# Performance work log

Measured on AMD Instinct MI355X. Metric: run time of the kernel, lower is better.

Reference implementation:

```python
import jax, jax.numpy as jnp
import numpy as np

B, L, C, H, W = 2, 3, 64, 32, 32
DI, N, DT_RANK, K = 128, 16, 4, 4  # d_inner=2*C, d_state, dt_rank=ceil(C/16), 4 scan dirs


def setup_inputs() -> dict:
    key = jax.random.key(0)
    ks = iter(jax.random.split(key, 48))
    nrm = lambda shape, s=0.02: jax.random.normal(next(ks), shape, jnp.float32) * s
    return {
        "image_sequence": jax.random.normal(next(ks), (B, L, C, H, W), jnp.float32),
        "difficult_zone": jax.random.normal(next(ks), (B, C, H, W), jnp.float32),
        "sigma": jax.random.uniform(next(ks), (B, C, H, W), jnp.float32),
        # LayerNorm2d applied to each frame
        "norm_g": jnp.ones((C,)), "norm_b": jnp.zeros((C,)),
        # ConvolutionalResBlock (in=3C -> out=C), GroupNorm(num_groups=1)
        "gn1_g": jnp.ones((3 * C,)), "gn1_b": jnp.zeros((3 * C,)),
        "conv1_w": nrm((C, 3 * C, 3, 3)), "conv1_b": jnp.zeros((C,)),
        "gn2_g": jnp.ones((C,)), "gn2_b": jnp.zeros((C,)),
        "conv2_w": nrm((C, C, 3, 3)), "conv2_b": jnp.zeros((C,)),
        "skip_w": nrm((C, 3 * C, 1, 1)), "skip_b": jnp.zeros((C,)),
        # VSSBlock pre-norms
        "ln1_g": jnp.ones((C,)), "ln1_b": jnp.zeros((C,)),
        "ln2_g": jnp.ones((C,)), "ln2_b": jnp.zeros((C,)),
        # SS2D
        "in_proj_w": nrm((2 * DI, C)),
        "dwconv_w": nrm((DI, 1, 3, 3)), "dwconv_b": jnp.zeros((DI,)),
        "x_proj_w": nrm((K, DT_RANK + 2 * N, DI)),
        "dt_proj_w": nrm((K, DI, DT_RANK), 0.1),
        "dt_proj_b": jnp.log(jnp.expm1(jnp.full((K, DI), 0.01, jnp.float32))),
        "A_logs": jnp.log(jnp.tile(jnp.arange(1, N + 1, dtype=jnp.float32), (K * DI, 1))),
        "Ds": jnp.ones((K * DI,)),
        "out_norm_g": jnp.ones((DI,)), "out_norm_b": jnp.zeros((DI,)),
        "out_proj_w": nrm((C, DI)),
        # Mlp (hidden = C)
        "fc1_w": nrm((C, C)), "fc1_b": jnp.zeros((C,)),
        "fc2_w": nrm((C, C)), "fc2_b": jnp.zeros((C,)),
    }


def _ln(x, g, b, eps=1e-5):  # layernorm over last axis
    m = x.mean(-1, keepdims=True)
    v = x.var(-1, keepdims=True)
    return (x - m) * jax.lax.rsqrt(v + eps) * g + b


def _ln2d(x, g, b, eps=1e-6):  # per-pixel channel layernorm, NCHW
    m = x.mean(1, keepdims=True)
    v = x.var(1, keepdims=True)
    return (x - m) * jax.lax.rsqrt(v + eps) * g[None, :, None, None] + b[None, :, None, None]


def _gn1(x, g, b, eps=1e-5):  # GroupNorm(num_groups=1), NCHW
    m = x.mean((1, 2, 3), keepdims=True)
    v = x.var((1, 2, 3), keepdims=True)
    return (x - m) * jax.lax.rsqrt(v + eps) * g[None, :, None, None] + b[None, :, None, None]


def _conv(x, w, b, pad):
    y = jax.lax.conv_general_dilated(x, w, (1, 1), [(pad, pad), (pad, pad)],
                                     dimension_numbers=("NCHW", "OIHW", "NCHW"))
    return y + b[None, :, None, None]


def _forward(image_sequence, difficult_zone, sigma, norm_g, norm_b, gn1_g, gn1_b,
             conv1_w, conv1_b, gn2_g, gn2_b, conv2_w, conv2_b, skip_w, skip_b,
             ln1_g, ln1_b, ln2_g, ln2_b, in_proj_w, dwconv_w, dwconv_b, x_proj_w,
             dt_proj_w, dt_proj_b, A_logs, Ds, out_norm_g, out_norm_b, out_proj_w,
             fc1_w, fc1_b, fc2_w, fc2_b):
    b, l, c, h, w = image_sequence.shape
    bl, L2 = b * l, h * w
    # fold frame loop into batch (identical math per frame in the torch loop)
    frames = _ln2d(image_sequence.reshape(bl, c, h, w), norm_g, norm_b)
    dz = jnp.broadcast_to(difficult_zone[:, None], (b, l, c, h, w)).reshape(bl, c, h, w)
    sg = jnp.broadcast_to(sigma[:, None], (b, l, c, h, w)).reshape(bl, c, h, w)
    x = jnp.concatenate([dz, frames, sg], axis=1)  # [bl, 3c, h, w]
    # channel compressor: pre-act conv res block
    hdn = _conv(jax.nn.silu(_gn1(x, gn1_g, gn1_b)), conv1_w, conv1_b, 1)
    hdn = _conv(jax.nn.silu(_gn1(hdn, gn2_g, gn2_b)), conv2_w, conv2_b, 1)
    x = hdn + _conv(x, skip_w, skip_b, 0)          # [bl, c, h, w]
    x = x.transpose(0, 2, 3, 1)                    # [bl, h, w, c]
    # --- VSSBlock (pre-norm): x = x + SS2D(LN(x)) ---
    xn = _ln(x, ln1_g, ln1_b)
    xz = xn @ in_proj_w.T                          # [bl,h,w,2*DI]
    xc, z = jnp.split(xz, 2, axis=-1)
    xc = xc.transpose(0, 3, 1, 2)                  # [bl, DI, h, w]
    xc = jax.lax.conv_general_dilated(xc, dwconv_w, (1, 1), [(1, 1), (1, 1)],
                                      dimension_numbers=("NCHW", "OIHW", "NCHW"),
                                      feature_group_count=DI) + dwconv_b[None, :, None, None]
    xc = jax.nn.silu(xc)
    # 4-direction scan inputs (HW, WH, and their reverses)
    xf = xc.reshape(bl, DI, L2)
    xt = xc.transpose(0, 1, 3, 2).reshape(bl, DI, L2)
    xs = jnp.stack([xf, xt], axis=1)
    xs = jnp.concatenate([xs, jnp.flip(xs, axis=-1)], axis=1)  # [bl, 4, DI, L2]
    x_dbl = jnp.einsum("bkdl,kcd->bkcl", xs, x_proj_w)
    dts, Bs, Cs = jnp.split(x_dbl, [DT_RANK, DT_RANK + N], axis=2)
    dts = jnp.einsum("bkrl,kdr->bkdl", dts, dt_proj_w) + dt_proj_b[None, :, :, None]
    dts = jax.nn.softplus(dts)                     # [bl, 4, DI, L2]
    A = -jnp.exp(A_logs).reshape(K, DI, N)
    dA = jnp.exp(dts[..., None] * A[None, :, :, None, :])            # [bl,4,DI,L2,N]
    dBu = dts[..., None] * Bs.transpose(0, 1, 3, 2)[:, :, None] * xs[..., None]
    a_t = dA.transpose(3, 0, 1, 2, 4)              # [L2, bl, 4, DI, N]
    bu_t = dBu.transpose(3, 0, 1, 2, 4)
    c_t = Cs.transpose(3, 0, 1, 2)                 # [L2, bl, 4, N]

    def step(hid, inp):
        a_i, bu_i, c_i = inp
        hid = a_i * hid + bu_i
        return hid, jnp.einsum("bkdn,bkn->bkd", hid, c_i)

    h0 = jnp.zeros((bl, K, DI, N), xs.dtype)
    _, ys = jax.lax.scan(step, h0, (a_t, bu_t, c_t))                 # [L2, bl, 4, DI]
    ys = ys.transpose(1, 2, 3, 0) + xs * Ds.reshape(K, DI)[None, :, :, None]
    inv = jnp.flip(ys[:, 2:4], axis=-1)
    y = (ys[:, 0] + inv[:, 0]
         + ys[:, 1].reshape(bl, DI, w, h).transpose(0, 1, 3, 2).reshape(bl, DI, L2)
         + inv[:, 1].reshape(bl, DI, w, h).transpose(0, 1, 3, 2).reshape(bl, DI, L2))
    y = _ln(y.transpose(0, 2, 1), out_norm_g, out_norm_b).reshape(bl, h, w, DI)
    y = y * jax.nn.silu(z)
    x = x + y @ out_proj_w.T
    # --- x = x + Mlp(LN(x)) ---
    xn = _ln(x, ln2_g, ln2_b)
    x = x + (jax.nn.gelu(xn @ fc1_w.T + fc1_b, approximate=False) @ fc2_w.T + fc2_b)
    return x.transpose(0, 3, 1, 2).reshape(b, l, c, h, w)


def reference(image_sequence, difficult_zone, sigma, norm_g, norm_b, gn1_g, gn1_b,
              conv1_w, conv1_b, gn2_g, gn2_b, conv2_w, conv2_b, skip_w, skip_b,
              ln1_g, ln1_b, ln2_g, ln2_b, in_proj_w, dwconv_w, dwconv_b, x_proj_w,
              dt_proj_w, dt_proj_b, A_logs, Ds, out_norm_g, out_norm_b, out_proj_w,
              fc1_w, fc1_b, fc2_w, fc2_b):
    return _forward(image_sequence, difficult_zone, sigma, norm_g, norm_b, gn1_g, gn1_b,
                    conv1_w, conv1_b, gn2_g, gn2_b, conv2_w, conv2_b, skip_w, skip_b,
                    ln1_g, ln1_b, ln2_g, ln2_b, in_proj_w, dwconv_w, dwconv_b, x_proj_w,
                    dt_proj_w, dt_proj_b, A_logs, Ds, out_norm_g, out_norm_b, out_proj_w,
                    fc1_w, fc1_b, fc2_w, fc2_b)
```

## Files before the change

### kernel.cpp

```cpp
#include <hip/hip_runtime.h>
#include <math.h>

#define BL    6
#define CCH   64
#define C3    192
#define L2    1024
#define DIC   128
#define NST   16
#define K4    4
#define PSTR  1088
#define NCH   32

#define LOG2E 1.44269504088896340736f
#define LN2C  0.69314718055994530942f

__device__ __forceinline__ float fexp(float x){ return __builtin_amdgcn_exp2f(x*LOG2E); }
__device__ __forceinline__ float fsilu(float x){ return x / (1.f + fexp(-x)); }
__device__ __forceinline__ float fsoftplus(float x){
  if (x > 20.f) return x;
  return __builtin_amdgcn_logf(1.f + fexp(x)) * LN2C;
}
__device__ __forceinline__ float fgelu(float x){
  return 0.5f*x*(1.f + erff(x*0.70710678118654752440f));
}

__global__ __launch_bounds__(256) void k_ln2d(const float* __restrict__ img,
    const float* __restrict__ dz, const float* __restrict__ sg,
    const float* __restrict__ g, const float* __restrict__ b, float* __restrict__ x3c,
    float* __restrict__ psum1, float* __restrict__ psq1){
  __shared__ float ps[4][64], pq[4][64];
  int s = blockIdx.x >> 4;
  int lane = threadIdx.x & 63;
  int cg = threadIdx.x >> 6;
  int p = ((blockIdx.x & 15) << 6) + lane;
  int bsmp = s/3;
  const float* fr = img + (size_t)s*CCH*L2;
  float vals[16]; float sm=0.f, sq=0.f;
  #pragma unroll
  for (int j=0;j<16;++j){
    int c = cg*16+j;
    float v = fr[c*L2+p];
    vals[j]=v; sm+=v; sq+=v*v;
  }
  ps[cg][lane]=sm; pq[cg][lane]=sq;
  __syncthreads();
  sm = ps[0][lane]+ps[1][lane]+ps[2][lane]+ps[3][lane];
  sq = pq[0][lane]+pq[1][lane]+pq[2][lane]+pq[3][lane];
  float mean = sm*(1.f/CCH); float var = sq*(1.f/CCH) - mean*mean;
  float rs = rsqrtf(var + 1e-6f);
  float* o = x3c + (size_t)s*C3*L2;
  const float* dzp = dz + (size_t)bsmp*CCH*L2;
  const float* sgp = sg + (size_t)bsmp*CCH*L2;
  float gsm=0.f, gsq=0.f;
  #pragma unroll
  for (int j=0;j<16;++j){
    int c = cg*16+j;
    float dzv = dzp[c*L2+p];
    float nv  = (vals[j]-mean)*rs*g[c] + b[c];
    float sgv = sgp[c*L2+p];
    o[c*L2+p] = dzv;
    o[(CCH+c)*L2+p] = nv;
    o[(2*CCH+c)*L2+p] = sgv;
    gsm += dzv+nv+sgv; gsq += dzv*dzv+nv*nv+sgv*sgv;
  }
  for (int m=1;m<64;m<<=1){ gsm+=__shfl_xor(gsm,m,64); gsq+=__shfl_xor(gsq,m,64); }
  __syncthreads();
  if (lane==0){ ps[cg][0]=gsm; pq[cg][0]=gsq; }
  __syncthreads();
  if (threadIdx.x==0){
    atomicAdd(psum1+s, ps[0][0]+ps[1][0]+ps[2][0]+ps[3][0]);
    atomicAdd(psq1 +s, pq[0][0]+pq[1][0]+pq[2][0]+pq[3][0]);
  }
}

__global__ __launch_bounds__(256) void k_gnact_pad(const float* __restrict__ x,
    const float* __restrict__ psum, const float* __restrict__ psq,
    const float* __restrict__ g, const float* __restrict__ b,
    int ch, float inv_n, float eps, float* __restrict__ out){
  int bx = blockIdx.x;
  int s = bx / ch; int c = bx % ch;
  int tid = threadIdx.x;
  float mean = psum[s]*inv_n;
  float var = psq[s]*inv_n - mean*mean;
  float rs = rsqrtf(var + eps);
  float gc = g[c]*rs; float bc = b[c] - mean*rs*g[c];
  float4 v = *(const float4*)(x + (size_t)bx*1024 + tid*4);
  float4 o; o.x = fsilu(v.x*gc+bc); o.y = fsilu(v.y*gc+bc);
  o.z = fsilu(v.z*gc+bc); o.w = fsilu(v.w*gc+bc);
  float* pl = out + (size_t)bx*PSTR;
  *(float4*)(pl + 32 + tid*4) = o;
  float4 z4 = make_float4(0.f,0.f,0.f,0.f);
  if (tid < 8)  *(float4*)(pl + tid*4) = z4;
  else if (tid < 16) *(float4*)(pl + 1056 + (tid-8)*4) = z4;
}

__device__ __forceinline__ void conv_row_acc(float4& a0, float4& a1, float4 mid, float lf, float rt,
    const float* wp0, const float* wp1){
  float w0=wp0[0], w1=wp0[1], w2=wp0[2];
  a0.x = fmaf(w0,lf,   fmaf(w1,mid.x, fmaf(w2,mid.y, a0.x)));
  a0.y = fmaf(w0,mid.x,fmaf(w1,mid.y, fmaf(w2,mid.z, a0.y)));
  a0.z = fmaf(w0,mid.y,fmaf(w1,mid.z, fmaf(w2,mid.w, a0.z)));
  a0.w = fmaf(w0,mid.z,fmaf(w1,mid.w, fmaf(w2,rt,    a0.w)));
  float v0=wp1[0], v1=wp1[1], v2=wp1[2];
  a1.x = fmaf(v0,lf,   fmaf(v1,mid.x, fmaf(v2,mid.y, a1.x)));
  a1.y = fmaf(v0,mid.x,fmaf(v1,mid.y, fmaf(v2,mid.z, a1.y)));
  a1.z = fmaf(v0,mid.y,fmaf(v1,mid.z, fmaf(v2,mid.w, a1.z)));
  a1.w = fmaf(v0,mid.z,fmaf(v1,mid.w, fmaf(v2,rt,    a1.w)));
}

__device__ __forceinline__ void conv_ci_body(float4 m0, float4 m1, float4 m2, int q,
    const float* wp0, const float* wp1, float4& a0, float4& a1){
  float lf0=__shfl_up(m0.w,1,64), rt0=__shfl_down(m0.x,1,64);
  float lf1=__shfl_up(m1.w,1,64), rt1=__shfl_down(m1.x,1,64);
  float lf2=__shfl_up(m2.w,1,64), rt2=__shfl_down(m2.x,1,64);
  if (q==0){ lf0=0.f; lf1=0.f; lf2=0.f; }
  if (q==7){ rt0=0.f; rt1=0.f; rt2=0.f; }
  conv_row_acc(a0,a1,m0,lf0,rt0, wp0+0, wp1+0);
  conv_row_acc(a0,a1,m1,lf1,rt1, wp0+3, wp1+3);
  conv_row_acc(a0,a1,m2,lf2,rt2, wp0+6, wp1+6);
}

__global__ __launch_bounds__(256) void k_conv1_split(const float* __restrict__ xact,
    const float* __restrict__ w, float* __restrict__ part){
  int bx = blockIdx.x; int kk = bx&7; int cop=(bx>>3)&31; int s=bx>>8;
  int co0 = cop*2, co1 = co0+1;
  int tid = threadIdx.x; int row = tid>>3; int q = tid&7; int col0 = q*4;
  float4 a0 = make_float4(0.f,0.f,0.f,0.f);
  float4 a1 = make_float4(0.f,0.f,0.f,0.f);
  int ci0 = kk*24;
  const float* pl = xact + ((size_t)s*C3 + ci0)*PSTR + row*32 + col0;
  const float* wp0 = w + (size_t)(co0*C3 + ci0)*9;
  const float* wp1 = w + (size_t)(co1*C3 + ci0)*9;
  float4 m0 = *(const float4*)(pl);
  float4 m1 = *(const float4*)(pl+32);
  float4 m2 = *(const float4*)(pl+64);
  #pragma unroll 2
  for (int i=0;i<24;++i){
    const float* pn = pl + (i<23 ? PSTR : 0);
    float4 n0 = *(const float4*)(pn);
    float4 n1 = *(const float4*)(pn+32);
    float4 n2 = *(const float4*)(pn+64);
    conv_ci_body(m0,m1,m2,q, wp0, wp1, a0, a1);
    wp0 += 9; wp1 += 9; pl = pn; m0=n0; m1=n1; m2=n2;
  }
  float* pp = part + (size_t)kk*(BL*CCH*L2) + ((size_t)s*CCH+co0)*L2 + row*32+col0;
  *(float4*)pp = a0;
  *(float4*)(pp+L2) = a1;
}

__global__ __launch_bounds__(256) void k_reduce1(const float* __restrict__ part,
    const float* __restrict__ bias, float* __restrict__ h1,
    float* __restrict__ psum2, float* __restrict__ psq2){
  int co = blockIdx.x & 63; int s = blockIdx.x >> 6;
  size_t ofs = ((size_t)s*CCH+co)*L2 + threadIdx.x*4;
  const size_t stride = (size_t)BL*CCH*L2;
  float4 acc = *(const float4*)(part + ofs);
  #pragma unroll
  for (int kk=1;kk<8;++kk){
    float4 r = *(const float4*)(part + (size_t)kk*stride + ofs);
    acc.x += r.x; acc.y += r.y; acc.z += r.z; acc.w += r.w;
  }
  float bv = bias[co];
  acc.x += bv; acc.y += bv; acc.z += bv; acc.w += bv;
  *(float4*)(h1 + ofs) = acc;
  float sm = acc.x+acc.y+acc.z+acc.w;
  float sq = acc.x*acc.x+acc.y*acc.y+acc.z*acc.z+acc.w*acc.w;
  for (int m=1;m<64;m<<=1){ sm+=__shfl_xor(sm,m,64); sq+=__shfl_xor(sq,m,64); }
  __shared__ float s_sm[4], s_sq[4];
  int wv = threadIdx.x>>6;
  if ((threadIdx.x&63)==0){ s_sm[wv]=sm; s_sq[wv]=sq; }
  __syncthreads();
  if (threadIdx.x==0){
    atomicAdd(psum2+s, s_sm[0]+s_sm[1]+s_sm[2]+s_sm[3]);
    atomicAdd(psq2 +s, s_sq[0]+s_sq[1]+s_sq[2]+s_sq[3]);
  }
}

__global__ __launch_bounds__(256) void k_conv2_split(const float* __restrict__ xact2,
    const float* __restrict__ x3c, const float* __restrict__ w2,
    const float* __restrict__ wsk, float* __restrict__ part){
  int t = blockIdx.x; int role = t % 3; t /= 3;
  int cop = t & 31; int s = t >> 5;
  int co0 = cop*2, co1 = co0+1;
  int tid = threadIdx.x; int row = tid>>3; int q = tid&7; int col0 = q*4;
  int p = row*32+col0;
  float4 a0 = make_float4(0.f,0.f,0.f,0.f);
  float4 a1 = make_float4(0.f,0.f,0.f,0.f);
  if (role < 2){
    int ci0 = role*32;
    const float* pl = xact2 + ((size_t)s*CCH + ci0)*PSTR + row*32 + col0;
    const float* wp0 = w2 + (size_t)(co0*CCH + ci0)*9;
    const float* wp1 = w2 + (size_t)(co1*CCH + ci0)*9;
    float4 m0 = *(const float4*)(pl);
    float4 m1 = *(const float4*)(pl+32);
    float4 m2 = *(const float4*)(pl+64);
    #pragma unroll 2
    for (int i=0;i<32;++i){
      const float* pn = pl + (i<31 ? PSTR : 0);
      float4 n0 = *(const float4*)(pn);
      float4 n1 = *(const float4*)(pn+32);
      float4 n2 = *(const float4*)(pn+64);
      conv_ci_body(m0,m1,m2,q, wp0, wp1, a0, a1);
      wp0 += 9; wp1 += 9; pl = pn; m0=n0; m1=n1; m2=n2;
    }
  } else {
    const float* x3 = x3c + (size_t)s*C3*L2 + p;
    #pragma unroll 4
    for (int ci=0; ci<C3; ++ci){
      float4 v = *(const float4*)(x3 + (size_t)ci*L2);
      float ws0 = wsk[co0*C3+ci], ws1 = wsk[co1*C3+ci];
      a0.x = fmaf(ws0,v.x,a0.x); a0.y = fmaf(ws0,v.y,a0.y); a0.z = fmaf(ws0,v.z,a0.z); a0.w = fmaf(ws0,v.w,a0.w);
      a1.x = fmaf(ws1,v.x,a1.x); a1.y = fmaf(ws1,v.y,a1.y); a1.z = fmaf(ws1,v.z,a1.z); a1.w = fmaf(ws1,v.w,a1.w);
    }
  }
  float* pp = part + (size_t)role*(BL*CCH*L2) + ((size_t)s*CCH+co0)*L2 + p;
  *(float4*)pp = a0;
  *(float4*)(pp+L2) = a1;
}

__global__ __launch_bounds__(256) void k_reduce2(const float* __restrict__ part,
    const float* __restrict__ b2, const float* __restrict__ bsk,
    float* __restrict__ xp, float* __restrict__ x_cmaj){
  int co = blockIdx.x & 63; int s = blockIdx.x >> 6;
  int p = threadIdx.x*4;
  size_t ofs = ((size_t)s*CCH+co)*L2 + p;
  const size_t stride = (size_t)BL*CCH*L2;
  float4 r0 = *(const float4*)(part + ofs);
  float4 r1 = *(const float4*)(part + stride + ofs);
  float4 r2 = *(const float4*)(part + 2*stride + ofs);
  float bv = b2[co]+bsk[co];
  float4 o;
  o.x = r0.x+r1.x+r2.x+bv;
  o.y = r0.y+r1.y+r2.y+bv;
  o.z = r0.z+r1.z+r2.z+bv;
  o.w = r0.w+r1.w+r2.w+bv;
  *(float4*)(x_cmaj + ofs) = o;
  float* xpb = xp + ((size_t)s*L2 + p)*CCH + co;
  xpb[0] = o.x; xpb[CCH] = o.y; xpb[2*CCH] = o.z; xpb[3*CCH] = o.w;
}

__global__ __launch_bounds__(256) void k_ln1_inproj(const float* __restrict__ xp,
    const float* __restrict__ g, const float* __restrict__ b, const float* __restrict__ W,
    float* __restrict__ xc, float* __restrict__ z_t){
  __shared__ float xn_s[64*65];
  int bx = blockIdx.x; int oq = bx & 3; int pg = (bx>>2)&15; int s = bx>>6;
  int p0 = pg*64;
  int tid = threadIdx.x; int wv = __builtin_amdgcn_readfirstlane(tid>>6); int lane = tid&63;
  for (int j=0;j<16;++j){
    int pl = wv*16 + j; int p = p0 + pl;
    float v = xp[((size_t)s*L2 + p)*CCH + lane];
    float sm = v, sq = v*v;
    for (int m=1;m<64;m<<=1){ sm += __shfl_xor(sm,m,64); sq += __shfl_xor(sq,m,64); }
    float mean = sm*(1.f/64.f); float var = sq*(1.f/64.f) - mean*mean;
    float rs = rsqrtf(var + 1e-5f);
    xn_s[pl*65 + lane] = (v-mean)*rs*g[lane] + b[lane];
  }
  __syncthreads();
  int px_l = tid & 63;
  int og = __builtin_amdgcn_readfirstlane(tid >> 6);
  int o0 = oq*64 + og*16;
  float acc[16];
  #pragma unroll
  for (int oi=0;oi<16;++oi) acc[oi]=0.f;
  for (int c=0;c<64;++c){
    float xv = xn_s[px_l*65 + c];
    #pragma unroll
    for (int oi=0;oi<16;++oi) acc[oi] = fmaf(W[(o0+oi)*64 + c], xv, acc[oi]);
  }
  int p = p0 + px_l;
  if (oq < 2){
    #pragma unroll
    for (int oi=0;oi<16;++oi) xc[((size_t)s*DIC + o0 + oi)*L2 + p] = acc[oi];
  } else {
    #pragma unroll
    for (int oi=0;oi<16;++oi) z_t[((size_t)s*DIC + (o0-128) + oi)*L2 + p] = acc[oi];
  }
}

__global__ __launch_bounds__(256) void k_dwconv(const float* __restrict__ xc,
    const float* __restrict__ w, const float* __restrict__ bias, float* __restrict__ xconv){
  int bx = blockIdx.x; int dch = bx & 127; int s = bx >> 7;
  int tid = threadIdx.x; int row = tid>>3; int q = tid&7; int col0 = q*4;
  const float* xr = xc + ((size_t)s*DIC+dch)*L2;
  const float* wp = w + dch*9;
  float bv = bias[dch];
  float4 acc = make_float4(bv,bv,bv,bv);
  #pragma unroll
  for (int dy=-1;dy<=1;++dy){
    int r = row+dy;
    float4 mid = make_float4(0.f,0.f,0.f,0.f);
    if (0<=r && r<32) mid = *(const float4*)(xr + r*32 + col0);
    float lf = __shfl_up(mid.w,1,64); if(q==0) lf=0.f;
    float rt = __shfl_down(mid.x,1,64); if(q==7) rt=0.f;
    float w0=wp[(dy+1)*3], w1=wp[(dy+1)*3+1], w2=wp[(dy+1)*3+2];
    acc.x = fmaf(w0,lf,   fmaf(w1,mid.x, fmaf(w2,mid.y, acc.x)));
    acc.y = fmaf(w0,mid.x,fmaf(w1,mid.y, fmaf(w2,mid.z, acc.y)));
    acc.z = fmaf(w0,mid.y,fmaf(w1,mid.z, fmaf(w2,mid.w, acc.z)));
    acc.w = fmaf(w0,mid.z,fmaf(w1,mid.w, fmaf(w2,rt,    acc.w)));
  }
  acc.x = fsilu(acc.x); acc.y = fsilu(acc.y); acc.z = fsilu(acc.z); acc.w = fsilu(acc.w);
  *(float4*)(xconv + ((size_t)s*DIC+dch)*L2 + row*32+col0) = acc;
}

__global__ __launch_bounds__(256) void k_xproj_dt(const float* __restrict__ xconv,
    const float* __restrict__ W, const float* __restrict__ dtw, const float* __restrict__ dtb,
    float* __restrict__ dtp, float* __restrict__ Bp, float* __restrict__ Cp,
    float* __restrict__ u_t){
  __shared__ float smem[128*68];
  int bx = blockIdx.x; int pg = bx & 15; int sk = bx >> 4;
  int k = sk & 3; int s = sk >> 2;
  int tid = threadIdx.x;
  for (int i = tid; i < 128*16; i += 256){
    int dr = i>>4; int j4 = (i&15)*4;
    float4 v = *(const float4*)(xconv + ((size_t)(s*DIC + dr))*L2 + pg*64 + j4);
    *(float4*)&smem[dr*68 + j4] = v;
  }
  __syncthreads();
  if (k == 0){
    float* ub = u_t + ((size_t)(s*L2) + pg*64)*DIC;
    for (int i = tid; i < 64*128; i += 256){
      int px2 = i>>7; int dd = i&127;
      ub[(size_t)px2*DIC + dd] = smem[dd*68 + px2];
    }
  }
  int px = tid & 63;
  int cgrp = __builtin_amdgcn_readfirstlane(tid >> 6);
  int c0 = cgrp*9;
  const float* wb = W + (size_t)(k*36 + c0)*DIC;
  float acc[9];
  #pragma unroll
  for (int ci=0;ci<9;++ci) acc[ci]=0.f;
  for (int d=0; d<DIC; ++d){
    float xv = smem[d*68 + px];
    #pragma unroll
    for (int ci=0;ci<9;++ci) acc[ci] = fmaf(wb[ci*DIC+d], xv, acc[ci]);
  }
  __syncthreads();
  #pragma unroll
  for (int ci=0;ci<9;++ci) smem[(c0+ci)*68 + px] = acc[ci];
  __syncthreads();
  int d = tid & 127; int half = tid >> 7;
  float w0 = dtw[(k*DIC+d)*4+0], w1 = dtw[(k*DIC+d)*4+1];
  float w2 = dtw[(k*DIC+d)*4+2], w3 = dtw[(k*DIC+d)*4+3];
  float bb = dtb[k*DIC+d];
  float* dout = dtp + ((size_t)sk*L2 + pg*64)*DIC + d;
  for (int pp = half*32; pp < half*32+32; ++pp){
    float r0 = smem[0*68+pp], r1 = smem[1*68+pp], r2 = smem[2*68+pp], r3 = smem[3*68+pp];
    float val = fsoftplus(fmaf(w0,r0,fmaf(w1,r1,fmaf(w2,r2,fmaf(w3,r3,bb)))));
    dout[(size_t)pp*DIC] = val;
  }
  float* Bb = Bp + ((size_t)sk*L2 + pg*64)*NST;
  float* Cb = Cp + ((size_t)sk*L2 + pg*64)*NST;
  for (int i = tid; i < 1024; i += 256){
    int pp = i>>4; int n = i&15;
    Bb[pp*NST + n] = smem[(4+n)*68 + pp];
    Cb[pp*NST + n] = smem[(20+n)*68 + pp];
  }
}

__device__ __forceinline__ int scan_pix32(int ch, int j, int k){
  if (k==0) return ch*32 + j;
  if (k==1) return j*32 + ch;
  if (k==2) return 1023 - (ch*32 + j);
  return 1023 - (j*32 + ch);
}

struct StepB { float dtv, uv; float4 B0,B1,B2,B3; };
__device__ __forceinline__ StepB loadB(const float* db, const float* ub, const float* Bb, int p){
  StepB r;
  r.dtv = db[(size_t)p*DIC]; r.uv = ub[(size_t)p*DIC];
  const float* bp = Bb + p*NST;
  r.B0 = *(const float4*)bp; r.B1 = *(const float4*)(bp+4);
  r.B2 = *(const float4*)(bp+8); r.B3 = *(const float4*)(bp+12);
  return r;
}

__global__ __launch_bounds__(256,2) void k_scan_part3(const float* __restrict__ dtp,
    const float* __restrict__ u_t, const float* __restrict__ Bp,
    const float* __restrict__ A_logs, float* __restrict__ hend, float* __restrict__ prodA){
  int bx = blockIdx.x; int chp = bx & 15; int sk = bx >> 4;
  int k = sk & 3; int s = sk >> 2;
  int tid = threadIdx.x; int d = tid & 127; int ch = chp*2 + (tid>>7);
  float aco[16];
  {
    const float* ab = A_logs + (size_t)(k*DIC+d)*NST;
    #pragma unroll
    for (int n=0;n<16;++n) aco[n] = -LOG2E * fexp(ab[n]);
  }
  float h[16], Pr[16];
  #pragma unroll
  for (int n=0;n<16;++n){ h[n]=0.f; Pr[n]=1.f; }
  const float* db = dtp + (size_t)sk*L2*DIC + d;
  const float* ub = u_t + (size_t)s*L2*DIC + d;
  const float* Bb = Bp + (size_t)sk*L2*NST;
  StepB cur = loadB(db, ub, Bb, scan_pix32(ch, 0, k));
  #pragma unroll 4
  for (int j=0;j<32;++j){
    StepB nxt;
    if (j < 31) nxt = loadB(db, ub, Bb, scan_pix32(ch, j+1, k));
    float tv = cur.dtv*cur.uv;
    #define PSTEP(NI, BV) { float a_ = __builtin_amdgcn_exp2f(cur.dtv*aco[NI]); \
      h[NI] = fmaf(a_, h[NI], tv*(BV)); Pr[NI] *= a_; }
    PSTEP(0,cur.B0.x) PSTEP(1,cur.B0.y) PSTEP(2,cur.B0.z) PSTEP(3,cur.B0.w)
    PSTEP(4,cur.B1.x) PSTEP(5,cur.B1.y) PSTEP(6,cur.B1.z) PSTEP(7,cur.B1.w)
    PSTEP(8,cur.B2.x) PSTEP(9,cur.B2.y) PSTEP(10,cur.B2.z) PSTEP(11,cur.B2.w)
    PSTEP(12,cur.B3.x) PSTEP(13,cur.B3.y) PSTEP(14,cur.B3.z) PSTEP(15,cur.B3.w)
    #undef PSTEP
    cur = nxt;
  }
  size_t base = ((size_t)(sk*NCH + ch)*DIC + d)*NST;
  #pragma unroll
  for (int q4=0;q4<4;++q4){
    *(float4*)(hend + base + q4*4)  = make_float4(h[q4*4],h[q4*4+1],h[q4*4+2],h[q4*4+3]);
    *(float4*)(prodA + base + q4*4) = make_float4(Pr[q4*4],Pr[q4*4+1],Pr[q4*4+2],Pr[q4*4+3]);
  }
}

__global__ __launch_bounds__(256) void k_scan_fix3(const float* __restrict__ hend,
    float* prodA_Hin){
  int t = blockIdx.x*256 + threadIdx.x;
  int n = t & 15; int d = (t>>4) & 127; int sk = t >> 11;
  float H = 0.f;
  for (int ch=0; ch<NCH; ++ch){
    size_t idx = ((size_t)(sk*NCH + ch)*DIC + d)*NST + n;
    float pa = prodA_Hin[idx];
    float he = hend[idx];
    prodA_Hin[idx] = H;
    H = fmaf(pa, H, he);
  }
}

__global__ __launch_bounds__(256,2) void k_scan_y3(const float* __restrict__ dtp,
    const float* __restrict__ u_t, const float* __restrict__ Bp, const float* __restrict__ Cp,
    const float* __restrict__ A_logs, const float* __restrict__ Ds,
    const float* __restrict__ Hin, float* __restrict__ ys_t){
  int bx = blockIdx.x; int chp = bx & 15; int sk = bx >> 4;
  int k = sk & 3; int s = sk >> 2;
  int tid = threadIdx.x; int d = tid & 127; int ch = chp*2 + (tid>>7);
  float aco[16];
  {
    const float* ab = A_logs + (size_t)(k*DIC+d)*NST;
    #pragma unroll
    for (int n=0;n<16;++n) aco[n] = -LOG2E * fexp(ab[n]);
  }
  float Dv = Ds[k*DIC+d];
  float h[16];
  size_t hbase = ((size_t)(sk*NCH + ch)*DIC + d)*NST;
  #pragma unroll
  for (int q4=0;q4<4;++q4){
    float4 hv = *(const float4*)(Hin + hbase + q4*4);
    h[q4*4]=hv.x; h[q4*4+1]=hv.y; h[q4*4+2]=hv.z; h[q4*4+3]=hv.w;
  }
  const float* db = dtp + (size_t)sk*L2*DIC + d;
  const float* ub = u_t + (size_t)s*L2*DIC + d;
  const float* Bb = Bp + (size_t)sk*L2*NST;
  const float* Cb = Cp + (size_t)sk*L2*NST;
  float* yb = ys_t + (size_t)sk*L2*DIC + d;
  int pcur = scan_pix32(ch, 0, k);
  StepB cur = loadB(db, ub, Bb, pcur);
  float4 Cc0 = *(const float4*)(Cb + pcur*NST);
  float4 Cc1 = *(const float4*)(Cb + pcur*NST + 4);
  float4 Cc2 = *(const float4*)(Cb + pcur*NST + 8);
  float4 Cc3 = *(const float4*)(Cb + pcur*NST + 12);
  #pragma unroll 4
  for (int j=0;j<32;++j){
    StepB nxt; float4 Cn0, Cn1, Cn2, Cn3; int pn = pcur;
    if (j < 31){
      pn = scan_pix32(ch, j+1, k);
      nxt = loadB(db, ub, Bb, pn);
      Cn0 = *(const float4*)(Cb + pn*NST);
      Cn1 = *(const float4*)(Cb + pn*NST + 4);
      Cn2 = *(const float4*)(Cb + pn*NST + 8);
      Cn3 = *(const float4*)(Cb + pn*NST + 12);
    }
    float tv = cur.dtv*cur.uv;
    float y0=0.f, y1=0.f, y2=0.f, y3=0.f;
    #define YSTEP(NI, BV, CV, YA) { float a_ = __builtin_amdgcn_exp2f(cur.dtv*aco[NI]); \
      h[NI] = fmaf(a_, h[NI], tv*(BV)); YA = fmaf(h[NI], (CV), YA); }
    YSTEP(0,cur.B0.x,Cc0.x,y0) YSTEP(1,cur.B0.y,Cc0.y,y1) YSTEP(2,cur.B0.z,Cc0.z,y2) YSTEP(3,cur.B0.w,Cc0.w,y3)
    YSTEP(4,cur.B1.x,Cc1.x,y0) YSTEP(5,cur.B1.y,Cc1.y,y1) YSTEP(6,cur.B1.z,Cc1.z,y2) YSTEP(7,cur.B1.w,Cc1.w,y3)
    YSTEP(8,cur.B2.x,Cc2.x,y0) YSTEP(9,cur.B2.y,Cc2.y,y1) YSTEP(10,cur.B2.z,Cc2.z,y2) YSTEP(11,cur.B2.w,Cc2.w,y3)
    YSTEP(12,cur.B3.x,Cc3.x,y0) YSTEP(13,cur.B3.y,Cc3.y,y1) YSTEP(14,cur.B3.z,Cc3.z,y2) YSTEP(15,cur.B3.w,Cc3.w,y3)
    #undef YSTEP
    yb[(size_t)pcur*DIC] = fmaf(cur.uv, Dv, (y0+y1)+(y2+y3));
    cur = nxt; Cc0 = Cn0; Cc1 = Cn1; Cc2 = Cn2; Cc3 = Cn3; pcur = pn;
  }
}

__global__ __launch_bounds__(256) void k_combine_outproj(const float* __restrict__ ys_t,
    const float* __restrict__ z_t, const float* __restrict__ g, const float* __restrict__ b,
    const float* __restrict__ W, const float* __restrict__ x_cmaj, float* __restrict__ xv){
  __shared__ float yt[128*17];
  int s = blockIdx.x >> 6; int pg = blockIdx.x & 63;
  int tid = threadIdx.x;
  int wv = __builtin_amdgcn_readfirstlane(tid>>6); int lane = tid&63;
  int d0 = lane, d1 = lane+64;
  for (int i=0;i<4;++i){
    int px = i*4 + wv; int p = pg*16 + px;
    const float* yb = ys_t + ((size_t)(s*4)*L2 + p)*DIC;
    float ya = yb[d0] + yb[(size_t)L2*DIC + d0] + yb[(size_t)2*L2*DIC + d0] + yb[(size_t)3*L2*DIC + d0];
    float yc = yb[d1] + yb[(size_t)L2*DIC + d1] + yb[(size_t)2*L2*DIC + d1] + yb[(size_t)3*L2*DIC + d1];
    float sm = ya+yc, sq = ya*ya+yc*yc;
    for (int m=1;m<64;m<<=1){ sm+=__shfl_xor(sm,m,64); sq+=__shfl_xor(sq,m,64); }
    float mean = sm*(1.f/128.f); float var = sq*(1.f/128.f)-mean*mean;
    float rs = rsqrtf(var + 1e-5f);
    float yn0 = (ya-mean)*rs*g[d0] + b[d0];
    float yn1 = (yc-mean)*rs*g[d1] + b[d1];
    float zv0 = z_t[((size_t)s*DIC+d0)*L2 + p];
    float zv1 = z_t[((size_t)s*DIC+d1)*L2 + p];
    yt[d0*17 + px] = yn0 * fsilu(zv0);
    yt[d1*17 + px] = yn1 * fsilu(zv1);
  }
  __syncthreads();
  int px = tid & 15; int cg = tid >> 4;
  int c0 = cg*4;
  float a0=0.f,a1=0.f,a2=0.f,a3=0.f;
  for (int d=0; d<DIC; ++d){
    float yv = yt[d*17 + px];
    a0 = fmaf(W[(c0+0)*DIC + d], yv, a0);
    a1 = fmaf(W[(c0+1)*DIC + d], yv, a1);
    a2 = fmaf(W[(c0+2)*DIC + d], yv, a2);
    a3 = fmaf(W[(c0+3)*DIC + d], yv, a3);
  }
  int p = pg*16 + px;
  size_t base = ((size_t)s*CCH + c0)*L2 + p;
  xv[base]      = x_cmaj[base]      + a0;
  xv[base+L2]   = x_cmaj[base+L2]   + a1;
  xv[base+2*L2] = x_cmaj[base+2*L2] + a2;
  xv[base+3*L2] = x_cmaj[base+3*L2] + a3;
}

__global__ __launch_bounds__(256) void k_mlp(const float* __restrict__ xv_in,
    const float* __restrict__ g, const float* __restrict__ b,
    const float* __restrict__ w1, const float* __restrict__ b1,
    const float* __restrict__ w2, const float* __restrict__ b2, float* __restrict__ out){
  __shared__ float xt[64*33];
  __shared__ float ts[32*65];
  int s = blockIdx.x >> 5; int p0 = (blockIdx.x & 31)*32;
  int tid = threadIdx.x; int px = tid & 31; int cg = tid >> 5;
  #pragma unroll
  for (int j=0;j<8;++j){
    int c = cg*8 + j;
    xt[c*33 + px] = xv_in[((size_t)s*CCH + c)*L2 + p0 + px];
  }
  __syncthreads();
  float sm=0.f, sq=0.f;
  for (int c=0;c<64;++c){ float v = xt[c*33+px]; sm+=v; sq+=v*v; }
  float mean = sm*(1.f/64.f);
  float rs = rsqrtf(sq*(1.f/64.f) - mean*mean + 1e-5f);
  int o0 = cg*8;
  float t[8];
  #pragma unroll
  for (int oi=0;oi<8;++oi) t[oi] = b1[o0+oi];
  for (int c=0;c<64;++c){
    float xn = (xt[c*33+px]-mean)*rs*g[c] + b[c];
    #pragma unroll
    for (int oi=0;oi<8;++oi) t[oi] = fmaf(xn, w1[(o0+oi)*64 + c], t[oi]);
  }
  #pragma unroll
  for (int oi=0;oi<8;++oi) ts[px*65 + o0+oi] = fgelu(t[oi]);
  __syncthreads();
  int c0 = cg*8;
  float acc[8];
  #pragma unroll
  for (int ci=0;ci<8;++ci) acc[ci] = xt[(c0+ci)*33+px] + b2[c0+ci];
  for (int o=0;o<64;++o){
    float tv = ts[px*65 + o];
    #pragma unroll
    for (int ci=0;ci<8;++ci) acc[ci] = fmaf(tv, w2[(c0+ci)*64 + o], acc[ci]);
  }
  #pragma unroll
  for (int ci=0;ci<8;++ci) out[((size_t)s*CCH + c0+ci)*L2 + p0 + px] = acc[ci];
}

extern "C" void kernel_launch(void* const* d_in, const int* in_sizes, int n_in,
                              void* d_out, int out_size, void* d_ws, size_t ws_size,
                              hipStream_t stream){
  (void)in_sizes; (void)n_in; (void)out_size; (void)ws_size;
  const float* img      = (const float*)d_in[0];
  const float* dz       = (const float*)d_in[1];
  const float* sg       = (const float*)d_in[2];
  const float* norm_g   = (const float*)d_in[3];
  const float* norm_b   = (const float*)d_in[4];
  const float* gn1_g    = (const float*)d_in[5];
  const float* gn1_b    = (const float*)d_in[6];
  const float* conv1_w  = (const float*)d_in[7];
  const float* conv1_b  = (const float*)d_in[8];
  const float* gn2_g    = (const float*)d_in[9];
  const float* gn2_b    = (const float*)d_in[10];
  const float* conv2_w  = (const float*)d_in[11];
  const float* conv2_b  = (const float*)d_in[12];
  const float* skip_w   = (const float*)d_in[13];
  const float* skip_b   = (const float*)d_in[14];
  const float* ln1_g    = (const float*)d_in[15];
  const float* ln1_b    = (const float*)d_in[16];
  const float* ln2_g    = (const float*)d_in[17];
  const float* ln2_b    = (const float*)d_in[18];
  const float* in_proj_w= (const float*)d_in[19];
  const float* dwconv_w = (const float*)d_in[20];
  const float* dwconv_b = (const float*)d_in[21];
  const float* x_proj_w = (const float*)d_in[22];
  const float* dt_proj_w= (const float*)d_in[23];
  const float* dt_proj_b= (const float*)d_in[24];
  const float* A_logs   = (const float*)d_in[25];
  const float* Ds       = (const float*)d_in[26];
  const float* out_norm_g = (const float*)d_in[27];
  const float* out_norm_b = (const float*)d_in[28];
  const float* out_proj_w = (const float*)d_in[29];
  const float* fc1_w    = (const float*)d_in[30];
  const float* fc1_b    = (const float*)d_in[31];
  const float* fc2_w    = (const float*)d_in[32];
  const float* fc2_b    = (const float*)d_in[33];

  float* ws = (float*)d_ws;
  float* x3c    = ws;
  float* xact1  = x3c    + 1179648;
  float* h1     = xact1  + 1253376;
  float* xact2  = h1     + 393216;
  float* xp     = xact2  + 417792;
  float* x_cmaj = xp     + 393216;
  float* z_t    = x_cmaj + 393216;
  float* xc     = z_t    + 786432;
  float* xconv  = xc     + 786432;
  float* hole   = xconv  + 786432;
  float* dtp    = hole   + 884736;
  float* ys_t   = dtp    + 3145728;
  float* xv     = ys_t   + 3145728;
  float* statsb = xv     + 393216;
  float* psum1  = statsb;
  float* psq1   = statsb + 6;
  float* psum2  = statsb + 12;
  float* psq2   = statsb + 18;
  float* part1  = dtp;
  float* part2  = ys_t;
  float* hend   = x3c;
  float* prodA  = xconv;
  float* u_t    = h1;
  float* Bp     = xp;
  float* Cp     = xc;

  hipMemsetAsync(statsb, 0, 24*sizeof(float), stream);
  k_ln2d<<<96, 256, 0, stream>>>(img, dz, sg, norm_g, norm_b, x3c, psum1, psq1);
  k_gnact_pad<<<6*C3, 256, 0, stream>>>(x3c, psum1, psq1, gn1_g, gn1_b, C3,
                                        1.f/(C3*L2), 1e-5f, xact1);
  k_conv1_split<<<1536, 256, 0, stream>>>(xact1, conv1_w, part1);
  k_reduce1<<<384, 256, 0, stream>>>(part1, conv1_b, h1, psum2, psq2);
  k_gnact_pad<<<6*CCH, 256, 0, stream>>>(h1, psum2, psq2, gn2_g, gn2_b, CCH,
                                         1.f/(CCH*L2), 1e-5f, xact2);
  k_conv2_split<<<576, 256, 0, stream>>>(xact2, x3c, conv2_w, skip_w, part2);
  k_reduce2<<<384, 256, 0, stream>>>(part2, conv2_b, skip_b, xp, x_cmaj);
  k_ln1_inproj<<<384, 256, 0, stream>>>(xp, ln1_g, ln1_b, in_proj_w, xc, z_t);
  k_dwconv<<<768, 256, 0, stream>>>(xc, dwconv_w, dwconv_b, xconv);
  k_xproj_dt<<<384, 256, 0, stream>>>(xconv, x_proj_w, dt_proj_w, dt_proj_b, dtp, Bp, Cp, u_t);
  k_scan_part3<<<384, 256, 0, stream>>>(dtp, u_t, Bp, A_logs, hend, prodA);
  k_scan_fix3<<<192, 256, 0, stream>>>(hend, prodA);
  k_scan_y3<<<384, 256, 0, stream>>>(dtp, u_t, Bp, Cp, A_logs, Ds, prodA, ys_t);
  k_combine_outproj<<<384, 256, 0, stream>>>(ys_t, z_t, out_norm_g, out_norm_b,
                                             out_proj_w, x_cmaj, xv);
  k_mlp<<<192, 256, 0, stream>>>(xv, ln2_g, ln2_b, fc1_w, fc1_b, fc2_w, fc2_b, (float*)d_out);
}
```

Measured before the change: 316.8 us.

## Fuse all stages into one cooperative persistent kernel with grid syncs

Turns every stage function into a device function and runs them all from a single cooperative mega-kernel. Each stage loops over its virtual blocks, and stages are separated by grid-wide barriers, with the grid capped at 512 blocks. The aim is to remove the launch overhead and inter-kernel gaps of fifteen launches. In exchange, every stage gets the same register and LDS footprint and fewer resident blocks, and grid.sync itself has a cost. If the cooperative launch fails, the code falls back to per-stage kernels.

```diff
diff --git a/kernel.cpp b/kernel.cpp
--- a/kernel.cpp
+++ b/kernel.cpp
@@ -1,5 +1,8 @@
 #include <hip/hip_runtime.h>
+#include <hip/hip_cooperative_groups.h>
 #include <math.h>
+
+namespace cg = cooperative_groups;
 
 #define BL    6
 #define CCH   64
@@ -24,75 +27,17 @@
   return 0.5f*x*(1.f + erff(x*0.70710678118654752440f));
 }
 
-__global__ __launch_bounds__(256) void k_ln2d(const float* __restrict__ img,
-    const float* __restrict__ dz, const float* __restrict__ sg,
-    const float* __restrict__ g, const float* __restrict__ b, float* __restrict__ x3c,
-    float* __restrict__ psum1, float* __restrict__ psq1){
-  __shared__ float ps[4][64], pq[4][64];
-  int s = blockIdx.x >> 4;
-  int lane = threadIdx.x & 63;
-  int cg = threadIdx.x >> 6;
-  int p = ((blockIdx.x & 15) << 6) + lane;
-  int bsmp = s/3;
-  const float* fr = img + (size_t)s*CCH*L2;
-  float vals[16]; float sm=0.f, sq=0.f;
-  #pragma unroll
-  for (int j=0;j<16;++j){
-    int c = cg*16+j;
-    float v = fr[c*L2+p];
-    vals[j]=v; sm+=v; sq+=v*v;
-  }
-  ps[cg][lane]=sm; pq[cg][lane]=sq;
-  __syncthreads();
-  sm = ps[0][lane]+ps[1][lane]+ps[2][lane]+ps[3][lane];
-  sq = pq[0][lane]+pq[1][lane]+pq[2][lane]+pq[3][lane];
-  float mean = sm*(1.f/CCH); float var = sq*(1.f/CCH) - mean*mean;
-  float rs = rsqrtf(var + 1e-6f);
-  float* o = x3c + (size_t)s*C3*L2;
-  const float* dzp = dz + (size_t)bsmp*CCH*L2;
-  const float* sgp = sg + (size_t)bsmp*CCH*L2;
-  float gsm=0.f, gsq=0.f;
-  #pragma unroll
-  for (int j=0;j<16;++j){
-    int c = cg*16+j;
-    float dzv = dzp[c*L2+p];
-    float nv  = (vals[j]-mean)*rs*g[c] + b[c];
-    float sgv = sgp[c*L2+p];
-    o[c*L2+p] = dzv;
-    o[(CCH+c)*L2+p] = nv;
-    o[(2*CCH+c)*L2+p] = sgv;
-    gsm += dzv+nv+sgv; gsq += dzv*dzv+nv*nv+sgv*sgv;
-  }
-  for (int m=1;m<64;m<<=1){ gsm+=__shfl_xor(gsm,m,64); gsq+=__shfl_xor(gsq,m,64); }
-  __syncthreads();
-  if (lane==0){ ps[cg][0]=gsm; pq[cg][0]=gsq; }
-  __syncthreads();
-  if (threadIdx.x==0){
-    atomicAdd(psum1+s, ps[0][0]+ps[1][0]+ps[2][0]+ps[3][0]);
-    atomicAdd(psq1 +s, pq[0][0]+pq[1][0]+pq[2][0]+pq[3][0]);
-  }
-}
-
-__global__ __launch_bounds__(256) void k_gnact_pad(const float* __restrict__ x,
-    const float* __restrict__ psum, const float* __restrict__ psq,
-    const float* __restrict__ g, const float* __restrict__ b,
-    int ch, float inv_n, float eps, float* __restrict__ out){
-  int bx = blockIdx.x;
-  int s = bx / ch; int c = bx % ch;
-  int tid = threadIdx.x;
-  float mean = psum[s]*inv_n;
-  float var = psq[s]*inv_n - mean*mean;
-  float rs = rsqrtf(var + eps);
-  float gc = g[c]*rs; float bc = b[c] - mean*rs*g[c];
-  float4 v = *(const float4*)(x + (size_t)bx*1024 + tid*4);
-  float4 o; o.x = fsilu(v.x*gc+bc); o.y = fsilu(v.y*gc+bc);
-  o.z = fsilu(v.z*gc+bc); o.w = fsilu(v.w*gc+bc);
-  float* pl = out + (size_t)bx*PSTR;
-  *(float4*)(pl + 32 + tid*4) = o;
-  float4 z4 = make_float4(0.f,0.f,0.f,0.f);
-  if (tid < 8)  *(float4*)(pl + tid*4) = z4;
-  else if (tid < 16) *(float4*)(pl + 1056 + (tid-8)*4) = z4;
-}
+struct MegaP {
+  const float *img,*dz,*sg,*norm_g,*norm_b,*gn1_g,*gn1_b,*conv1_w,*conv1_b,
+              *gn2_g,*gn2_b,*conv2_w,*conv2_b,*skip_w,*skip_b,*ln1_g,*ln1_b,
+              *ln2_g,*ln2_b,*in_proj_w,*dwconv_w,*dwconv_b,*x_proj_w,
+              *dt_proj_w,*dt_proj_b,*A_logs,*Ds,*out_norm_g,*out_norm_b,
+              *out_proj_w,*fc1_w,*fc1_b,*fc2_w,*fc2_b;
+  float *x3c,*xact1,*h1,*xact2,*xp,*x_cmaj,*z_t,*xc,*xconv,*dtp,*ys_t,*xv;
+  float *psum1,*psq1,*psum2,*psq2;
+  float *part1,*part2,*hend,*prodA,*u_t,*Bp,*Cp;
+  float *out;
+};
 
 __device__ __forceinline__ void conv_row_acc(float4& a0, float4& a1, float4 mid, float lf, float rt,
     const float* wp0, const float* wp1){
@@ -120,17 +65,100 @@
   conv_row_acc(a0,a1,m2,lf2,rt2, wp0+6, wp1+6);
 }
 
-__global__ __launch_bounds__(256) void k_conv1_split(const float* __restrict__ xact,
-    const float* __restrict__ w, float* __restrict__ part){
-  int bx = blockIdx.x; int kk = bx&7; int cop=(bx>>3)&31; int s=bx>>8;
+__device__ __forceinline__ int scan_pix32(int ch, int j, int k){
+  if (k==0) return ch*32 + j;
+  if (k==1) return j*32 + ch;
+  if (k==2) return 1023 - (ch*32 + j);
+  return 1023 - (j*32 + ch);
+}
+
+struct StepB { float dtv, uv; float4 B0,B1,B2,B3; };
+__device__ __forceinline__ StepB loadB(const float* db, const float* ub, const float* Bb, int p){
+  StepB r;
+  r.dtv = db[(size_t)p*DIC]; r.uv = ub[(size_t)p*DIC];
+  const float* bp = Bb + p*NST;
+  r.B0 = *(const float4*)bp; r.B1 = *(const float4*)(bp+4);
+  r.B2 = *(const float4*)(bp+8); r.B3 = *(const float4*)(bp+12);
+  return r;
+}
+
+
+__device__ __forceinline__ void p0_ln2d(int vb, int tid, const MegaP& P, float* smem){
+  float* ps = smem;
+  float* pq = smem + 256;
+  int s = vb >> 4;
+  int lane = tid & 63;
+  int cgp = tid >> 6;
+  int p = ((vb & 15) << 6) + lane;
+  int bsmp = s/3;
+  const float* fr = P.img + (size_t)s*CCH*L2;
+  float vals[16]; float sm=0.f, sq=0.f;
+  #pragma unroll
+  for (int j=0;j<16;++j){
+    int c = cgp*16+j;
+    float v = fr[c*L2+p];
+    vals[j]=v; sm+=v; sq+=v*v;
+  }
+  ps[cgp*64+lane]=sm; pq[cgp*64+lane]=sq;
+  __syncthreads();
+  sm = ps[lane]+ps[64+lane]+ps[128+lane]+ps[192+lane];
+  sq = pq[lane]+pq[64+lane]+pq[128+lane]+pq[192+lane];
+  float mean = sm*(1.f/CCH); float var = sq*(1.f/CCH) - mean*mean;
+  float rs = rsqrtf(var + 1e-6f);
+  float* o = P.x3c + (size_t)s*C3*L2;
+  const float* dzp = P.dz + (size_t)bsmp*CCH*L2;
+  const float* sgp = P.sg + (size_t)bsmp*CCH*L2;
+  float gsm=0.f, gsq=0.f;
+  #pragma unroll
+  for (int j=0;j<16;++j){
+    int c = cgp*16+j;
+    float dzv = dzp[c*L2+p];
+    float nv  = (vals[j]-mean)*rs*P.norm_g[c] + P.norm_b[c];
+    float sgv = sgp[c*L2+p];
+    o[c*L2+p] = dzv;
+    o[(CCH+c)*L2+p] = nv;
+    o[(2*CCH+c)*L2+p] = sgv;
+    gsm += dzv+nv+sgv; gsq += dzv*dzv+nv*nv+sgv*sgv;
+  }
+  for (int m=1;m<64;m<<=1){ gsm+=__shfl_xor(gsm,m,64); gsq+=__shfl_xor(gsq,m,64); }
+  __syncthreads();
+  if (lane==0){ ps[cgp*64]=gsm; pq[cgp*64]=gsq; }
+  __syncthreads();
+  if (tid==0){
+    atomicAdd(P.psum1+s, ps[0]+ps[64]+ps[128]+ps[192]);
+    atomicAdd(P.psq1 +s, pq[0]+pq[64]+pq[128]+pq[192]);
+  }
+}
+
+__device__ __forceinline__ void gnact_body(int vb, int tid, const float* __restrict__ x,
+    const float* __restrict__ psum, const float* __restrict__ psq,
+    const float* __restrict__ g, const float* __restrict__ b,
+    int ch, float inv_n, float eps, float* __restrict__ out){
+  int s = vb / ch; int c = vb % ch;
+  float mean = psum[s]*inv_n;
+  float var = psq[s]*inv_n - mean*mean;
+  float rs = rsqrtf(var + eps);
+  float gc = g[c]*rs; float bc = b[c] - mean*rs*g[c];
+  float4 v = *(const float4*)(x + (size_t)vb*1024 + tid*4);
+  float4 o; o.x = fsilu(v.x*gc+bc); o.y = fsilu(v.y*gc+bc);
+  o.z = fsilu(v.z*gc+bc); o.w = fsilu(v.w*gc+bc);
+  float* pl = out + (size_t)vb*PSTR;
+  *(float4*)(pl + 32 + tid*4) = o;
+  float4 z4 = make_float4(0.f,0.f,0.f,0.f);
+  if (tid < 8)  *(float4*)(pl + tid*4) = z4;
+  else if (tid < 16) *(float4*)(pl + 1056 + (tid-8)*4) = z4;
+}
+
+__device__ __forceinline__ void p2_conv1(int vb, int tid, const MegaP& P){
+  int kk = vb&7; int cop=(vb>>3)&31; int s=vb>>8;
   int co0 = cop*2, co1 = co0+1;
-  int tid = threadIdx.x; int row = tid>>3; int q = tid&7; int col0 = q*4;
+  int row = tid>>3; int q = tid&7; int col0 = q*4;
   float4 a0 = make_float4(0.f,0.f,0.f,0.f);
   float4 a1 = make_float4(0.f,0.f,0.f,0.f);
   int ci0 = kk*24;
-  const float* pl = xact + ((size_t)s*C3 + ci0)*PSTR + row*32 + col0;
-  const float* wp0 = w + (size_t)(co0*C3 + ci0)*9;
-  const float* wp1 = w + (size_t)(co1*C3 + ci0)*9;
+  const float* pl = P.xact1 + ((size_t)s*C3 + ci0)*PSTR + row*32 + col0;
+  const float* wp0 = P.conv1_w + (size_t)(co0*C3 + ci0)*9;
+  const float* wp1 = P.conv1_w + (size_t)(co1*C3 + ci0)*9;
   float4 m0 = *(const float4*)(pl);
   float4 m1 = *(const float4*)(pl+32);
   float4 m2 = *(const float4*)(pl+64);
@@ -143,54 +171,50 @@
     conv_ci_body(m0,m1,m2,q, wp0, wp1, a0, a1);
     wp0 += 9; wp1 += 9; pl = pn; m0=n0; m1=n1; m2=n2;
   }
-  float* pp = part + (size_t)kk*(BL*CCH*L2) + ((size_t)s*CCH+co0)*L2 + row*32+col0;
+  float* pp = P.part1 + (size_t)kk*(BL*CCH*L2) + ((size_t)s*CCH+co0)*L2 + row*32+col0;
   *(float4*)pp = a0;
   *(float4*)(pp+L2) = a1;
 }
 
-__global__ __launch_bounds__(256) void k_reduce1(const float* __restrict__ part,
-    const float* __restrict__ bias, float* __restrict__ h1,
-    float* __restrict__ psum2, float* __restrict__ psq2){
-  int co = blockIdx.x & 63; int s = blockIdx.x >> 6;
-  size_t ofs = ((size_t)s*CCH+co)*L2 + threadIdx.x*4;
+__device__ __forceinline__ void p3_reduce1(int vb, int tid, const MegaP& P, float* smem){
+  float* s_sm = smem; float* s_sq = smem+4;
+  int co = vb & 63; int s = vb >> 6;
+  size_t ofs = ((size_t)s*CCH+co)*L2 + tid*4;
   const size_t stride = (size_t)BL*CCH*L2;
-  float4 acc = *(const float4*)(part + ofs);
+  float4 acc = *(const float4*)(P.part1 + ofs);
   #pragma unroll
   for (int kk=1;kk<8;++kk){
-    float4 r = *(const float4*)(part + (size_t)kk*stride + ofs);
+    float4 r = *(const float4*)(P.part1 + (size_t)kk*stride + ofs);
     acc.x += r.x; acc.y += r.y; acc.z += r.z; acc.w += r.w;
   }
-  float bv = bias[co];
+  float bv = P.conv1_b[co];
   acc.x += bv; acc.y += bv; acc.z += bv; acc.w += bv;
-  *(float4*)(h1 + ofs) = acc;
+  *(float4*)(P.h1 + ofs) = acc;
   float sm = acc.x+acc.y+acc.z+acc.w;
   float sq = acc.x*acc.x+acc.y*acc.y+acc.z*acc.z+acc.w*acc.w;
   for (int m=1;m<64;m<<=1){ sm+=__shfl_xor(sm,m,64); sq+=__shfl_xor(sq,m,64); }
-  __shared__ float s_sm[4], s_sq[4];
-  int wv = threadIdx.x>>6;
-  if ((threadIdx.x&63)==0){ s_sm[wv]=sm; s_sq[wv]=sq; }
-  __syncthreads();
-  if (threadIdx.x==0){
-    atomicAdd(psum2+s, s_sm[0]+s_sm[1]+s_sm[2]+s_sm[3]);
-    atomicAdd(psq2 +s, s_sq[0]+s_sq[1]+s_sq[2]+s_sq[3]);
-  }
-}
-
-__global__ __launch_bounds__(256) void k_conv2_split(const float* __restrict__ xact2,
-    const float* __restrict__ x3c, const float* __restrict__ w2,
-    const float* __restrict__ wsk, float* __restrict__ part){
-  int t = blockIdx.x; int role = t % 3; t /= 3;
-  int cop = t & 31; int s = t >> 5;
+  int wv = tid>>6;
+  if ((tid&63)==0){ s_sm[wv]=sm; s_sq[wv]=sq; }
+  __syncthreads();
+  if (tid==0){
+    atomicAdd(P.psum2+s, s_sm[0]+s_sm[1]+s_sm[2]+s_sm[3]);
+    atomicAdd(P.psq2 +s, s_sq[0]+s_sq[1]+s_sq[2]+s_sq[3]);
+  }
+}
+
+__device__ __forceinline__ void p5_conv2(int vb, int tid, const MegaP& P){
+  int t2 = vb; int role = t2 % 3; t2 /= 3;
+  int cop = t2 & 31; int s = t2 >> 5;
   int co0 = cop*2, co1 = co0+1;
-  int tid = threadIdx.x; int row = tid>>3; int q = tid&7; int col0 = q*4;
+  int row = tid>>3; int q = tid&7; int col0 = q*4;
   int p = row*32+col0;
   float4 a0 = make_float4(0.f,0.f,0.f,0.f);
   float4 a1 = make_float4(0.f,0.f,0.f,0.f);
   if (role < 2){
     int ci0 = role*32;
-    const float* pl = xact2 + ((size_t)s*CCH + ci0)*PSTR + row*32 + col0;
-    const float* wp0 = w2 + (size_t)(co0*CCH + ci0)*9;
-    const float* wp1 = w2 + (size_t)(co1*CCH + ci0)*9;
+    const float* pl = P.xact2 + ((size_t)s*CCH + ci0)*PSTR + row*32 + col0;
+    const float* wp0 = P.conv2_w + (size_t)(co0*CCH + ci0)*9;
+    const float* wp1 = P.conv2_w + (size_t)(co1*CCH + ci0)*9;
     float4 m0 = *(const float4*)(pl);
     float4 m1 = *(const float4*)(pl+32);
     float4 m2 = *(const float4*)(pl+64);
@@ -204,56 +228,51 @@
       wp0 += 9; wp1 += 9; pl = pn; m0=n0; m1=n1; m2=n2;
     }
   } else {
-    const float* x3 = x3c + (size_t)s*C3*L2 + p;
+    const float* x3 = P.x3c + (size_t)s*C3*L2 + p;
     #pragma unroll 4
     for (int ci=0; ci<C3; ++ci){
       float4 v = *(const float4*)(x3 + (size_t)ci*L2);
-      float ws0 = wsk[co0*C3+ci], ws1 = wsk[co1*C3+ci];
+      float ws0 = P.skip_w[co0*C3+ci], ws1 = P.skip_w[co1*C3+ci];
       a0.x = fmaf(ws0,v.x,a0.x); a0.y = fmaf(ws0,v.y,a0.y); a0.z = fmaf(ws0,v.z,a0.z); a0.w = fmaf(ws0,v.w,a0.w);
       a1.x = fmaf(ws1,v.x,a1.x); a1.y = fmaf(ws1,v.y,a1.y); a1.z = fmaf(ws1,v.z,a1.z); a1.w = fmaf(ws1,v.w,a1.w);
     }
   }
-  float* pp = part + (size_t)role*(BL*CCH*L2) + ((size_t)s*CCH+co0)*L2 + p;
+  float* pp = P.part2 + (size_t)role*(BL*CCH*L2) + ((size_t)s*CCH+co0)*L2 + p;
   *(float4*)pp = a0;
   *(float4*)(pp+L2) = a1;
 }
 
-__global__ __launch_bounds__(256) void k_reduce2(const float* __restrict__ part,
-    const float* __restrict__ b2, const float* __restrict__ bsk,
-    float* __restrict__ xp, float* __restrict__ x_cmaj){
-  int co = blockIdx.x & 63; int s = blockIdx.x >> 6;
-  int p = threadIdx.x*4;
+__device__ __forceinline__ void p6_reduce2(int vb, int tid, const MegaP& P){
+  int co = vb & 63; int s = vb >> 6;
+  int p = tid*4;
   size_t ofs = ((size_t)s*CCH+co)*L2 + p;
   const size_t stride = (size_t)BL*CCH*L2;
-  float4 r0 = *(const float4*)(part + ofs);
-  float4 r1 = *(const float4*)(part + stride + ofs);
-  float4 r2 = *(const float4*)(part + 2*stride + ofs);
-  float bv = b2[co]+bsk[co];
+  float4 r0 = *(const float4*)(P.part2 + ofs);
+  float4 r1 = *(const float4*)(P.part2 + stride + ofs);
+  float4 r2 = *(const float4*)(P.part2 + 2*stride + ofs);
+  float bv = P.conv2_b[co]+P.skip_b[co];
   float4 o;
   o.x = r0.x+r1.x+r2.x+bv;
   o.y = r0.y+r1.y+r2.y+bv;
   o.z = r0.z+r1.z+r2.z+bv;
   o.w = r0.w+r1.w+r2.w+bv;
-  *(float4*)(x_cmaj + ofs) = o;
-  float* xpb = xp + ((size_t)s*L2 + p)*CCH + co;
+  *(float4*)(P.x_cmaj + ofs) = o;
+  float* xpb = P.xp + ((size_t)s*L2 + p)*CCH + co;
   xpb[0] = o.x; xpb[CCH] = o.y; xpb[2*CCH] = o.z; xpb[3*CCH] = o.w;
 }
 
-__global__ __launch_bounds__(256) void k_ln1_inproj(const float* __restrict__ xp,
-    const float* __restrict__ g, const float* __restrict__ b, const float* __restrict__ W,
-    float* __restrict__ xc, float* __restrict__ z_t){
-  __shared__ float xn_s[64*65];
-  int bx = blockIdx.x; int oq = bx & 3; int pg = (bx>>2)&15; int s = bx>>6;
+__device__ __forceinline__ void p7_ln1_inproj(int vb, int tid, const MegaP& P, float* xn_s){
+  int oq = vb & 3; int pg = (vb>>2)&15; int s = vb>>6;
   int p0 = pg*64;
-  int tid = threadIdx.x; int wv = __builtin_amdgcn_readfirstlane(tid>>6); int lane = tid&63;
+  int wv = __builtin_amdgcn_readfirstlane(tid>>6); int lane = tid&63;
   for (int j=0;j<16;++j){
     int pl = wv*16 + j; int p = p0 + pl;
-    float v = xp[((size_t)s*L2 + p)*CCH + lane];
+    float v = P.xp[((size_t)s*L2 + p)*CCH + lane];
     float sm = v, sq = v*v;
     for (int m=1;m<64;m<<=1){ sm += __shfl_xor(sm,m,64); sq += __shfl_xor(sq,m,64); }
     float mean = sm*(1.f/64.f); float var = sq*(1.f/64.f) - mean*mean;
     float rs = rsqrtf(var + 1e-5f);
-    xn_s[pl*65 + lane] = (v-mean)*rs*g[lane] + b[lane];
+    xn_s[pl*65 + lane] = (v-mean)*rs*P.ln1_g[lane] + P.ln1_b[lane];
   }
   __syncthreads();
   int px_l = tid & 63;
@@ -265,25 +284,24 @@
   for (int c=0;c<64;++c){
     float xv = xn_s[px_l*65 + c];
     #pragma unroll
-    for (int oi=0;oi<16;++oi) acc[oi] = fmaf(W[(o0+oi)*64 + c], xv, acc[oi]);
+    for (int oi=0;oi<16;++oi) acc[oi] = fmaf(P.in_proj_w[(o0+oi)*64 + c], xv, acc[oi]);
   }
   int p = p0 + px_l;
   if (oq < 2){
     #pragma unroll
-    for (int oi=0;oi<16;++oi) xc[((size_t)s*DIC + o0 + oi)*L2 + p] = acc[oi];
+    for (int oi=0;oi<16;++oi) P.xc[((size_t)s*DIC + o0 + oi)*L2 + p] = acc[oi];
   } else {
     #pragma unroll
-    for (int oi=0;oi<16;++oi) z_t[((size_t)s*DIC + (o0-128) + oi)*L2 + p] = acc[oi];
-  }
-}
-
-__global__ __launch_bounds__(256) void k_dwconv(const float* __restrict__ xc,
-    const float* __restrict__ w, const float* __restrict__ bias, float* __restrict__ xconv){
-  int bx = blockIdx.x; int dch = bx & 127; int s = bx >> 7;
-  int tid = threadIdx.x; int row = tid>>3; int q = tid&7; int col0 = q*4;
-  const float* xr = xc + ((size_t)s*DIC+dch)*L2;
-  const float* wp = w + dch*9;
-  float bv = bias[dch];
+    for (int oi=0;oi<16;++oi) P.z_t[((size_t)s*DIC + (o0-128) + oi)*L2 + p] = acc[oi];
+  }
+}
+
+__device__ __forceinline__ void p8_dwconv(int vb, int tid, const MegaP& P){
+  int dch = vb & 127; int s = vb >> 7;
+  int row = tid>>3; int q = tid&7; int col0 = q*4;
+  const float* xr = P.xc + ((size_t)s*DIC+dch)*L2;
+  const float* wp = P.dwconv_w + dch*9;
+  float bv = P.dwconv_b[dch];
   float4 acc = make_float4(bv,bv,bv,bv);
   #pragma unroll
   for (int dy=-1;dy<=1;++dy){
@@ -299,25 +317,20 @@
     acc.w = fmaf(w0,mid.z,fmaf(w1,mid.w, fmaf(w2,rt,    acc.w)));
   }
   acc.x = fsilu(acc.x); acc.y = fsilu(acc.y); acc.z = fsilu(acc.z); acc.w = fsilu(acc.w);
-  *(float4*)(xconv + ((size_t)s*DIC+dch)*L2 + row*32+col0) = acc;
-}
-
-__global__ __launch_bounds__(256) void k_xproj_dt(const float* __restrict__ xconv,
-    const float* __restrict__ W, const float* __restrict__ dtw, const float* __restrict__ dtb,
-    float* __restrict__ dtp, float* __restrict__ Bp, float* __restrict__ Cp,
-    float* __restrict__ u_t){
-  __shared__ float smem[128*68];
-  int bx = blockIdx.x; int pg = bx & 15; int sk = bx >> 4;
+  *(float4*)(P.xconv + ((size_t)s*DIC+dch)*L2 + row*32+col0) = acc;
+}
+
+__device__ __forceinline__ void p9_xproj_dt(int vb, int tid, const MegaP& P, float* smem){
+  int pg = vb & 15; int sk = vb >> 4;
   int k = sk & 3; int s = sk >> 2;
-  int tid = threadIdx.x;
   for (int i = tid; i < 128*16; i += 256){
     int dr = i>>4; int j4 = (i&15)*4;
-    float4 v = *(const float4*)(xconv + ((size_t)(s*DIC + dr))*L2 + pg*64 + j4);
+    float4 v = *(const float4*)(P.xconv + ((size_t)(s*DIC + dr))*L2 + pg*64 + j4);
     *(float4*)&smem[dr*68 + j4] = v;
   }
   __syncthreads();
   if (k == 0){
-    float* ub = u_t + ((size_t)(s*L2) + pg*64)*DIC;
+    float* ub = P.u_t + ((size_t)(s*L2) + pg*64)*DIC;
     for (int i = tid; i < 64*128; i += 256){
       int px2 = i>>7; int dd = i&127;
       ub[(size_t)px2*DIC + dd] = smem[dd*68 + px2];
@@ -326,7 +339,7 @@
   int px = tid & 63;
   int cgrp = __builtin_amdgcn_readfirstlane(tid >> 6);
   int c0 = cgrp*9;
-  const float* wb = W + (size_t)(k*36 + c0)*DIC;
+  const float* wb = P.x_proj_w + (size_t)(k*36 + c0)*DIC;
   float acc[9];
   #pragma unroll
   for (int ci=0;ci<9;++ci) acc[ci]=0.f;
@@ -340,17 +353,17 @@
   for (int ci=0;ci<9;++ci) smem[(c0+ci)*68 + px] = acc[ci];
   __syncthreads();
   int d = tid & 127; int half = tid >> 7;
-  float w0 = dtw[(k*DIC+d)*4+0], w1 = dtw[(k*DIC+d)*4+1];
-  float w2 = dtw[(k*DIC+d)*4+2], w3 = dtw[(k*DIC+d)*4+3];
-  float bb = dtb[k*DIC+d];
-  float* dout = dtp + ((size_t)sk*L2 + pg*64)*DIC + d;
+  float w0 = P.dt_proj_w[(k*DIC+d)*4+0], w1 = P.dt_proj_w[(k*DIC+d)*4+1];
+  float w2 = P.dt_proj_w[(k*DIC+d)*4+2], w3 = P.dt_proj_w[(k*DIC+d)*4+3];
+  float bb = P.dt_proj_b[k*DIC+d];
+  float* dout = P.dtp + ((size_t)sk*L2 + pg*64)*DIC + d;
   for (int pp = half*32; pp < half*32+32; ++pp){
     float r0 = smem[0*68+pp], r1 = smem[1*68+pp], r2 = smem[2*68+pp], r3 = smem[3*68+pp];
     float val = fsoftplus(fmaf(w0,r0,fmaf(w1,r1,fmaf(w2,r2,fmaf(w3,r3,bb)))));
     dout[(size_t)pp*DIC] = val;
   }
-  float* Bb = Bp + ((size_t)sk*L2 + pg*64)*NST;
-  float* Cb = Cp + ((size_t)sk*L2 + pg*64)*NST;
+  float* Bb = P.Bp + ((size_t)sk*L2 + pg*64)*NST;
+  float* Cb = P.Cp + ((size_t)sk*L2 + pg*64)*NST;
   for (int i = tid; i < 1024; i += 256){
     int pp = i>>4; int n = i&15;
     Bb[pp*NST + n] = smem[(4+n)*68 + pp];
@@ -358,41 +371,22 @@
   }
 }
 
-__device__ __forceinline__ int scan_pix32(int ch, int j, int k){
-  if (k==0) return ch*32 + j;
-  if (k==1) return j*32 + ch;
-  if (k==2) return 1023 - (ch*32 + j);
-  return 1023 - (j*32 + ch);
-}
-
-struct StepB { float dtv, uv; float4 B0,B1,B2,B3; };
-__device__ __forceinline__ StepB loadB(const float* db, const float* ub, const float* Bb, int p){
-  StepB r;
-  r.dtv = db[(size_t)p*DIC]; r.uv = ub[(size_t)p*DIC];
-  const float* bp = Bb + p*NST;
-  r.B0 = *(const float4*)bp; r.B1 = *(const float4*)(bp+4);
-  r.B2 = *(const float4*)(bp+8); r.B3 = *(const float4*)(bp+12);
-  return r;
-}
-
-__global__ __launch_bounds__(256,2) void k_scan_part3(const float* __restrict__ dtp,
-    const float* __restrict__ u_t, const float* __restrict__ Bp,
-    const float* __restrict__ A_logs, float* __restrict__ hend, float* __restrict__ prodA){
-  int bx = blockIdx.x; int chp = bx & 15; int sk = bx >> 4;
+__device__ __forceinline__ void p10_scan_part(int vb, int tid, const MegaP& P){
+  int chp = vb & 15; int sk = vb >> 4;
   int k = sk & 3; int s = sk >> 2;
-  int tid = threadIdx.x; int d = tid & 127; int ch = chp*2 + (tid>>7);
+  int d = tid & 127; int ch = chp*2 + (tid>>7);
   float aco[16];
   {
-    const float* ab = A_logs + (size_t)(k*DIC+d)*NST;
+    const float* ab = P.A_logs + (size_t)(k*DIC+d)*NST;
     #pragma unroll
     for (int n=0;n<16;++n) aco[n] = -LOG2E * fexp(ab[n]);
   }
   float h[16], Pr[16];
   #pragma unroll
   for (int n=0;n<16;++n){ h[n]=0.f; Pr[n]=1.f; }
-  const float* db = dtp + (size_t)sk*L2*DIC + d;
-  const float* ub = u_t + (size_t)s*L2*DIC + d;
-  const float* Bb = Bp + (size_t)sk*L2*NST;
+  const float* db = P.dtp + (size_t)sk*L2*DIC + d;
+  const float* ub = P.u_t + (size_t)s*L2*DIC + d;
+  const float* Bb = P.Bp + (size_t)sk*L2*NST;
   StepB cur = loadB(db, ub, Bb, scan_pix32(ch, 0, k));
   #pragma unroll 4
   for (int j=0;j<32;++j){
@@ -411,51 +405,47 @@
   size_t base = ((size_t)(sk*NCH + ch)*DIC + d)*NST;
   #pragma unroll
   for (int q4=0;q4<4;++q4){
-    *(float4*)(hend + base + q4*4)  = make_float4(h[q4*4],h[q4*4+1],h[q4*4+2],h[q4*4+3]);
-    *(float4*)(prodA + base + q4*4) = make_float4(Pr[q4*4],Pr[q4*4+1],Pr[q4*4+2],Pr[q4*4+3]);
-  }
-}
-
-__global__ __launch_bounds__(256) void k_scan_fix3(const float* __restrict__ hend,
-    float* prodA_Hin){
-  int t = blockIdx.x*256 + threadIdx.x;
+    *(float4*)(P.hend + base + q4*4)  = make_float4(h[q4*4],h[q4*4+1],h[q4*4+2],h[q4*4+3]);
+    *(float4*)(P.prodA + base + q4*4) = make_float4(Pr[q4*4],Pr[q4*4+1],Pr[q4*4+2],Pr[q4*4+3]);
+  }
+}
+
+__device__ __forceinline__ void p11_scan_fix(int vb, int tid, const MegaP& P){
+  int t = vb*256 + tid;
   int n = t & 15; int d = (t>>4) & 127; int sk = t >> 11;
   float H = 0.f;
   for (int ch=0; ch<NCH; ++ch){
     size_t idx = ((size_t)(sk*NCH + ch)*DIC + d)*NST + n;
-    float pa = prodA_Hin[idx];
-    float he = hend[idx];
-    prodA_Hin[idx] = H;
+    float pa = P.prodA[idx];
+    float he = P.hend[idx];
+    P.prodA[idx] = H;
     H = fmaf(pa, H, he);
   }
 }
 
-__global__ __launch_bounds__(256,2) void k_scan_y3(const float* __restrict__ dtp,
-    const float* __restrict__ u_t, const float* __restrict__ Bp, const float* __restrict__ Cp,
-    const float* __restrict__ A_logs, const float* __restrict__ Ds,
-    const float* __restrict__ Hin, float* __restrict__ ys_t){
-  int bx = blockIdx.x; int chp = bx & 15; int sk = bx >> 4;
+__device__ __forceinline__ void p12_scan_y(int vb, int tid, const MegaP& P){
+  int chp = vb & 15; int sk = vb >> 4;
   int k = sk & 3; int s = sk >> 2;
-  int tid = threadIdx.x; int d = tid & 127; int ch = chp*2 + (tid>>7);
+  int d = tid & 127; int ch = chp*2 + (tid>>7);
   float aco[16];
   {
-    const float* ab = A_logs + (size_t)(k*DIC+d)*NST;
+    const float* ab = P.A_logs + (size_t)(k*DIC+d)*NST;
     #pragma unroll
     for (int n=0;n<16;++n) aco[n] = -LOG2E * fexp(ab[n]);
   }
-  float Dv = Ds[k*DIC+d];
+  float Dv = P.Ds[k*DIC+d];
   float h[16];
   size_t hbase = ((size_t)(sk*NCH + ch)*DIC + d)*NST;
   #pragma unroll
   for (int q4=0;q4<4;++q4){
-    float4 hv = *(const float4*)(Hin + hbase + q4*4);
+    float4 hv = *(const float4*)(P.prodA + hbase + q4*4);
     h[q4*4]=hv.x; h[q4*4+1]=hv.y; h[q4*4+2]=hv.z; h[q4*4+3]=hv.w;
   }
-  const float* db = dtp + (size_t)sk*L2*DIC + d;
-  const float* ub = u_t + (size_t)s*L2*DIC + d;
-  const float* Bb = Bp + (size_t)sk*L2*NST;
-  const float* Cb = Cp + (size_t)sk*L2*NST;
-  float* yb = ys_t + (size_t)sk*L2*DIC + d;
+  const float* db = P.dtp + (size_t)sk*L2*DIC + d;
+  const float* ub = P.u_t + (size_t)s*L2*DIC + d;
+  const float* Bb = P.Bp + (size_t)sk*L2*NST;
+  const float* Cb = P.Cp + (size_t)sk*L2*NST;
+  float* yb = P.ys_t + (size_t)sk*L2*DIC + d;
   int pcur = scan_pix32(ch, 0, k);
   StepB cur = loadB(db, ub, Bb, pcur);
   float4 Cc0 = *(const float4*)(Cb + pcur*NST);
@@ -487,131 +477,158 @@
   }
 }
 
-__global__ __launch_bounds__(256) void k_combine_outproj(const float* __restrict__ ys_t,
-    const float* __restrict__ z_t, const float* __restrict__ g, const float* __restrict__ b,
-    const float* __restrict__ W, const float* __restrict__ x_cmaj, float* __restrict__ xv){
-  __shared__ float yt[128*17];
-  int s = blockIdx.x >> 6; int pg = blockIdx.x & 63;
-  int tid = threadIdx.x;
+__device__ __forceinline__ void p13_combine(int vb, int tid, const MegaP& P, float* yt){
+  int s = vb >> 6; int pg = vb & 63;
   int wv = __builtin_amdgcn_readfirstlane(tid>>6); int lane = tid&63;
   int d0 = lane, d1 = lane+64;
   for (int i=0;i<4;++i){
     int px = i*4 + wv; int p = pg*16 + px;
-    const float* yb = ys_t + ((size_t)(s*4)*L2 + p)*DIC;
+    const float* yb = P.ys_t + ((size_t)(s*4)*L2 + p)*DIC;
     float ya = yb[d0] + yb[(size_t)L2*DIC + d0] + yb[(size_t)2*L2*DIC + d0] + yb[(size_t)3*L2*DIC + d0];
     float yc = yb[d1] + yb[(size_t)L2*DIC + d1] + yb[(size_t)2*L2*DIC + d1] + yb[(size_t)3*L2*DIC + d1];
     float sm = ya+yc, sq = ya*ya+yc*yc;
     for (int m=1;m<64;m<<=1){ sm+=__shfl_xor(sm,m,64); sq+=__shfl_xor(sq,m,64); }
     float mean = sm*(1.f/128.f); float var = sq*(1.f/128.f)-mean*mean;
     float rs = rsqrtf(var + 1e-5f);
-    float yn0 = (ya-mean)*rs*g[d0] + b[d0];
-    float yn1 = (yc-mean)*rs*g[d1] + b[d1];
-    float zv0 = z_t[((size_t)s*DIC+d0)*L2 + p];
-    float zv1 = z_t[((size_t)s*DIC+d1)*L2 + p];
+    float yn0 = (ya-mean)*rs*P.out_norm_g[d0] + P.out_norm_b[d0];
+    float yn1 = (yc-mean)*rs*P.out_norm_g[d1] + P.out_norm_b[d1];
+    float zv0 = P.z_t[((size_t)s*DIC+d0)*L2 + p];
+    float zv1 = P.z_t[((size_t)s*DIC+d1)*L2 + p];
     yt[d0*17 + px] = yn0 * fsilu(zv0);
     yt[d1*17 + px] = yn1 * fsilu(zv1);
   }
   __syncthreads();
-  int px = tid & 15; int cg = tid >> 4;
-  int c0 = cg*4;
+  int px = tid & 15; int cgp = tid >> 4;
+  int c0 = cgp*4;
   float a0=0.f,a1=0.f,a2=0.f,a3=0.f;
   for (int d=0; d<DIC; ++d){
     float yv = yt[d*17 + px];
-    a0 = fmaf(W[(c0+0)*DIC + d], yv, a0);
-    a1 = fmaf(W[(c0+1)*DIC + d], yv, a1);
-    a2 = fmaf(W[(c0+2)*DIC + d], yv, a2);
-    a3 = fmaf(W[(c0+3)*DIC + d], yv, a3);
+    a0 = fmaf(P.out_proj_w[(c0+0)*DIC + d], yv, a0);
+    a1 = fmaf(P.out_proj_w[(c0+1)*DIC + d], yv, a1);
+    a2 = fmaf(P.out_proj_w[(c0+2)*DIC + d], yv, a2);
+    a3 = fmaf(P.out_proj_w[(c0+3)*DIC + d], yv, a3);
   }
   int p = pg*16 + px;
   size_t base = ((size_t)s*CCH + c0)*L2 + p;
-  xv[base]      = x_cmaj[base]      + a0;
-  xv[base+L2]   = x_cmaj[base+L2]   + a1;
-  xv[base+2*L2] = x_cmaj[base+2*L2] + a2;
-  xv[base+3*L2] = x_cmaj[base+3*L2] + a3;
-}
-
-__global__ __launch_bounds__(256) void k_mlp(const float* __restrict__ xv_in,
-    const float* __restrict__ g, const float* __restrict__ b,
-    const float* __restrict__ w1, const float* __restrict__ b1,
-    const float* __restrict__ w2, const float* __restrict__ b2, float* __restrict__ out){
-  __shared__ float xt[64*33];
-  __shared__ float ts[32*65];
-  int s = blockIdx.x >> 5; int p0 = (blockIdx.x & 31)*32;
-  int tid = threadIdx.x; int px = tid & 31; int cg = tid >> 5;
+  P.xv[base]      = P.x_cmaj[base]      + a0;
+  P.xv[base+L2]   = P.x_cmaj[base+L2]   + a1;
+  P.xv[base+2*L2] = P.x_cmaj[base+2*L2] + a2;
+  P.xv[base+3*L2] = P.x_cmaj[base+3*L2] + a3;
+}
+
+__device__ __forceinline__ void p14_mlp(int vb, int tid, const MegaP& P, float* smem){
+  float* xt = smem;
+  float* ts = smem + 2112;
+  int s = vb >> 5; int p0 = (vb & 31)*32;
+  int px = tid & 31; int cgp = tid >> 5;
   #pragma unroll
   for (int j=0;j<8;++j){
-    int c = cg*8 + j;
-    xt[c*33 + px] = xv_in[((size_t)s*CCH + c)*L2 + p0 + px];
+    int c = cgp*8 + j;
+    xt[c*33 + px] = P.xv[((size_t)s*CCH + c)*L2 + p0 + px];
   }
   __syncthreads();
   float sm=0.f, sq=0.f;
   for (int c=0;c<64;++c){ float v = xt[c*33+px]; sm+=v; sq+=v*v; }
   float mean = sm*(1.f/64.f);
   float rs = rsqrtf(sq*(1.f/64.f) - mean*mean + 1e-5f);
-  int o0 = cg*8;
+  int o0 = cgp*8;
   float t[8];
   #pragma unroll
-  for (int oi=0;oi<8;++oi) t[oi] = b1[o0+oi];
+  for (int oi=0;oi<8;++oi) t[oi] = P.fc1_b[o0+oi];
   for (int c=0;c<64;++c){
-    float xn = (xt[c*33+px]-mean)*rs*g[c] + b[c];
+    float xn = (xt[c*33+px]-mean)*rs*P.ln2_g[c] + P.ln2_b[c];
     #pragma unroll
-    for (int oi=0;oi<8;++oi) t[oi] = fmaf(xn, w1[(o0+oi)*64 + c], t[oi]);
+    for (int oi=0;oi<8;++oi) t[oi] = fmaf(xn, P.fc1_w[(o0+oi)*64 + c], t[oi]);
   }
   #pragma unroll
   for (int oi=0;oi<8;++oi) ts[px*65 + o0+oi] = fgelu(t[oi]);
   __syncthreads();
-  int c0 = cg*8;
+  int c0 = cgp*8;
   float acc[8];
   #pragma unroll
-  for (int ci=0;ci<8;++ci) acc[ci] = xt[(c0+ci)*33+px] + b2[c0+ci];
+  for (int ci=0;ci<8;++ci) acc[ci] = xt[(c0+ci)*33+px] + P.fc2_b[c0+ci];
   for (int o=0;o<64;++o){
     float tv = ts[px*65 + o];
     #pragma unroll
-    for (int ci=0;ci<8;++ci) acc[ci] = fmaf(tv, w2[(c0+ci)*64 + o], acc[ci]);
-  }
-  #pragma unroll
-  for (int ci=0;ci<8;++ci) out[((size_t)s*CCH + c0+ci)*L2 + p0 + px] = acc[ci];
+    for (int ci=0;ci<8;++ci) acc[ci] = fmaf(tv, P.fc2_w[(c0+ci)*64 + o], acc[ci]);
+  }
+  #pragma unroll
+  for (int ci=0;ci<8;++ci) P.out[((size_t)s*CCH + c0+ci)*L2 + p0 + px] = acc[ci];
+}
+
+__global__ __launch_bounds__(256,2) void k_mega(MegaP P){
+  cg::grid_group grd = cg::this_grid();
+  __shared__ float smem[8704];
+  const int tid = threadIdx.x;
+  for (int vb = blockIdx.x; vb < 96; vb += gridDim.x){ p0_ln2d(vb, tid, P, smem); __syncthreads(); }
+  grd.sync();
+  for (int vb = blockIdx.x; vb < 6*C3; vb += gridDim.x)
+    gnact_body(vb, tid, P.x3c, P.psum1, P.psq1, P.gn1_g, P.gn1_b, C3, 1.f/(C3*L2), 1e-5f, P.xact1);
+  grd.sync();
+  for (int vb = blockIdx.x; vb < 1536; vb += gridDim.x) p2_conv1(vb, tid, P);
+  grd.sync();
+  for (int vb = blockIdx.x; vb < 384; vb += gridDim.x){ p3_reduce1(vb, tid, P, smem); __syncthreads(); }
+  grd.sync();
+  for (int vb = blockIdx.x; vb < 6*CCH; vb += gridDim.x)
+    gnact_body(vb, tid, P.h1, P.psum2, P.psq2, P.gn2_g, P.gn2_b, CCH, 1.f/(CCH*L2), 1e-5f, P.xact2);
+  grd.sync();
+  for (int vb = blockIdx.x; vb < 576; vb += gridDim.x) p5_conv2(vb, tid, P);
+  grd.sync();
+  for (int vb = blockIdx.x; vb < 384; vb += gridDim.x) p6_reduce2(vb, tid, P);
+  grd.sync();
+  for (int vb = blockIdx.x; vb < 384; vb += gridDim.x){ p7_ln1_inproj(vb, tid, P, smem); __syncthreads(); }
+  grd.sync();
+  for (int vb = blockIdx.x; vb < 768; vb += gridDim.x) p8_dwconv(vb, tid, P);
+  grd.sync();
+  for (int vb = blockIdx.x; vb < 384; vb += gridDim.x){ p9_xproj_dt(vb, tid, P, smem); __syncthreads(); }
+  grd.sync();
+  for (int vb = blockIdx.x; vb < 384; vb += gridDim.x) p10_scan_part(vb, tid, P);
+  grd.sync();
+  for (int vb = blockIdx.x; vb < 192; vb += gridDim.x) p11_scan_fix(vb, tid, P);
+  grd.sync();
+  for (int vb = blockIdx.x; vb < 384; vb += gridDim.x) p12_scan_y(vb, tid, P);
+  grd.sync();
+  for (int vb = blockIdx.x; vb < 384; vb += gridDim.x){ p13_combine(vb, tid, P, smem); __syncthreads(); }
+  grd.sync();
+  for (int vb = blockIdx.x; vb < 192; vb += gridDim.x){ p14_mlp(vb, tid, P, smem); __syncthreads(); }
+}
+
+__global__ __launch_bounds__(256) void k_p0(MegaP P){
+  __shared__ float smem[512]; p0_ln2d(blockIdx.x, threadIdx.x, P, smem);
+}
+__global__ __launch_bounds__(256) void k_p1(MegaP P){
+  gnact_body(blockIdx.x, threadIdx.x, P.x3c, P.psum1, P.psq1, P.gn1_g, P.gn1_b, C3, 1.f/(C3*L2), 1e-5f, P.xact1);
+}
+__global__ __launch_bounds__(256) void k_p2(MegaP P){ p2_conv1(blockIdx.x, threadIdx.x, P); }
+__global__ __launch_bounds__(256) void k_p3(MegaP P){
+  __shared__ float smem[8]; p3_reduce1(blockIdx.x, threadIdx.x, P, smem);
+}
+__global__ __launch_bounds__(256) void k_p4(MegaP P){
+  gnact_body(blockIdx.x, threadIdx.x, P.h1, P.psum2, P.psq2, P.gn2_g, P.gn2_b, CCH, 1.f/(CCH*L2), 1e-5f, P.xact2);
+}
+__global__ __launch_bounds__(256) void k_p5(MegaP P){ p5_conv2(blockIdx.x, threadIdx.x, P); }
+__global__ __launch_bounds__(256) void k_p6(MegaP P){ p6_reduce2(blockIdx.x, threadIdx.x, P); }
+__global__ __launch_bounds__(256) void k_p7(MegaP P){
+  __shared__ float smem[64*65]; p7_ln1_inproj(blockIdx.x, threadIdx.x, P, smem);
+}
+__global__ __launch_bounds__(256) void k_p8(MegaP P){ p8_dwconv(blockIdx.x, threadIdx.x, P); }
+__global__ __launch_bounds__(256) void k_p9(MegaP P){
+  __shared__ float smem[8704]; p9_xproj_dt(blockIdx.x, threadIdx.x, P, smem);
+}
+__global__ __launch_bounds__(256,2) void k_p10(MegaP P){ p10_scan_part(blockIdx.x, threadIdx.x, P); }
+__global__ __launch_bounds__(256) void k_p11(MegaP P){ p11_scan_fix(blockIdx.x, threadIdx.x, P); }
+__global__ __launch_bounds__(256,2) void k_p12(MegaP P){ p12_scan_y(blockIdx.x, threadIdx.x, P); }
+__global__ __launch_bounds__(256) void k_p13(MegaP P){
+  __shared__ float smem[128*17]; p13_combine(blockIdx.x, threadIdx.x, P, smem);
+}
+__global__ __launch_bounds__(256) void k_p14(MegaP P){
+  __shared__ float smem[4192]; p14_mlp(blockIdx.x, threadIdx.x, P, smem);
 }
 
 extern "C" void kernel_launch(void* const* d_in, const int* in_sizes, int n_in,
                               void* d_out, int out_size, void* d_ws, size_t ws_size,
                               hipStream_t stream){
   (void)in_sizes; (void)n_in; (void)out_size; (void)ws_size;
-  const float* img      = (const float*)d_in[0];
-  const float* dz       = (const float*)d_in[1];
-  const float* sg       = (const float*)d_in[2];
-  const float* norm_g   = (const float*)d_in[3];
-  const float* norm_b   = (const float*)d_in[4];
-  const float* gn1_g    = (const float*)d_in[5];
-  const float* gn1_b    = (const float*)d_in[6];
-  const float* conv1_w  = (const float*)d_in[7];
-  const float* conv1_b  = (const float*)d_in[8];
-  const float* gn2_g    = (const float*)d_in[9];
-  const float* gn2_b    = (const float*)d_in[10];
-  const float* conv2_w  = (const float*)d_in[11];
-  const float* conv2_b  = (const float*)d_in[12];
-  const float* skip_w   = (const float*)d_in[13];
-  const float* skip_b   = (const float*)d_in[14];
-  const float* ln1_g    = (const float*)d_in[15];
-  const float* ln1_b    = (const float*)d_in[16];
-  const float* ln2_g    = (const float*)d_in[17];
-  const float* ln2_b    = (const float*)d_in[18];
-  const float* in_proj_w= (const float*)d_in[19];
-  const float* dwconv_w = (const float*)d_in[20];
-  const float* dwconv_b = (const float*)d_in[21];
-  const float* x_proj_w = (const float*)d_in[22];
-  const float* dt_proj_w= (const float*)d_in[23];
-  const float* dt_proj_b= (const float*)d_in[24];
-  const float* A_logs   = (const float*)d_in[25];
-  const float* Ds       = (const float*)d_in[26];
-  const float* out_norm_g = (const float*)d_in[27];
-  const float* out_norm_b = (const float*)d_in[28];
-  const float* out_proj_w = (const float*)d_in[29];
-  const float* fc1_w    = (const float*)d_in[30];
-  const float* fc1_b    = (const float*)d_in[31];
-  const float* fc2_w    = (const float*)d_in[32];
-  const float* fc2_b    = (const float*)d_in[33];
-
   float* ws = (float*)d_ws;
   float* x3c    = ws;
   float* xact1  = x3c    + 1179648;
@@ -627,35 +644,70 @@
   float* ys_t   = dtp    + 3145728;
   float* xv     = ys_t   + 3145728;
   float* statsb = xv     + 393216;
-  float* psum1  = statsb;
-  float* psq1   = statsb + 6;
-  float* psum2  = statsb + 12;
-  float* psq2   = statsb + 18;
-  float* part1  = dtp;
-  float* part2  = ys_t;
-  float* hend   = x3c;
-  float* prodA  = xconv;
-  float* u_t    = h1;
-  float* Bp     = xp;
-  float* Cp     = xc;
+
+  MegaP Pm;
+  Pm.img = (const float*)d_in[0];  Pm.dz = (const float*)d_in[1];
+  Pm.sg = (const float*)d_in[2];   Pm.norm_g = (const float*)d_in[3];
+  Pm.norm_b = (const float*)d_in[4]; Pm.gn1_g = (const float*)d_in[5];
+  Pm.gn1_b = (const float*)d_in[6]; Pm.conv1_w = (const float*)d_in[7];
+  Pm.conv1_b = (const float*)d_in[8]; Pm.gn2_g = (const float*)d_in[9];
+  Pm.gn2_b = (const float*)d_in[10]; Pm.conv2_w = (const float*)d_in[11];
+  Pm.conv2_b = (const float*)d_in[12]; Pm.skip_w = (const float*)d_in[13];
+  Pm.skip_b = (const float*)d_in[14]; Pm.ln1_g = (const float*)d_in[15];
+  Pm.ln1_b = (const float*)d_in[16]; Pm.ln2_g = (const float*)d_in[17];
+  Pm.ln2_b = (const float*)d_in[18]; Pm.in_proj_w = (const float*)d_in[19];
+  Pm.dwconv_w = (const float*)d_in[20]; Pm.dwconv_b = (const float*)d_in[21];
+  Pm.x_proj_w = (const float*)d_in[22]; Pm.dt_proj_w = (const float*)d_in[23];
+  Pm.dt_proj_b = (const float*)d_in[24]; Pm.A_logs = (const float*)d_in[25];
+  Pm.Ds = (const float*)d_in[26]; Pm.out_norm_g = (const float*)d_in[27];
+  Pm.out_norm_b = (const float*)d_in[28]; Pm.out_proj_w = (const float*)d_in[29];
+  Pm.fc1_w = (const float*)d_in[30]; Pm.fc1_b = (const float*)d_in[31];
+  Pm.fc2_w = (const float*)d_in[32]; Pm.fc2_b = (const float*)d_in[33];
+
+  Pm.x3c = x3c; Pm.xact1 = xact1; Pm.h1 = h1; Pm.xact2 = xact2; Pm.xp = xp;
+  Pm.x_cmaj = x_cmaj; Pm.z_t = z_t; Pm.xc = xc; Pm.xconv = xconv;
+  Pm.dtp = dtp; Pm.ys_t = ys_t; Pm.xv = xv;
+  Pm.psum1 = statsb; Pm.psq1 = statsb+6; Pm.psum2 = statsb+12; Pm.psq2 = statsb+18;
+  Pm.part1 = dtp;
+  Pm.part2 = ys_t;
+  Pm.hend  = x3c;
+  Pm.prodA = xconv;
+  Pm.u_t   = h1;
+  Pm.Bp    = xp;
+  Pm.Cp    = xc;
+  Pm.out   = (float*)d_out;
 
   hipMemsetAsync(statsb, 0, 24*sizeof(float), stream);
-  k_ln2d<<<96, 256, 0, stream>>>(img, dz, sg, norm_g, norm_b, x3c, psum1, psq1);
-  k_gnact_pad<<<6*C3, 256, 0, stream>>>(x3c, psum1, psq1, gn1_g, gn1_b, C3,
-                                        1.f/(C3*L2), 1e-5f, xact1);
-  k_conv1_split<<<1536, 256, 0, stream>>>(xact1, conv1_w, part1);
-  k_reduce1<<<384, 256, 0, stream>>>(part1, conv1_b, h1, psum2, psq2);
-  k_gnact_pad<<<6*CCH, 256, 0, stream>>>(h1, psum2, psq2, gn2_g, gn2_b, CCH,
-                                         1.f/(CCH*L2), 1e-5f, xact2);
-  k_conv2_split<<<576, 256, 0, stream>>>(xact2, x3c, conv2_w, skip_w, part2);
-  k_reduce2<<<384, 256, 0, stream>>>(part2, conv2_b, skip_b, xp, x_cmaj);
-  k_ln1_inproj<<<384, 256, 0, stream>>>(xp, ln1_g, ln1_b, in_proj_w, xc, z_t);
-  k_dwconv<<<768, 256, 0, stream>>>(xc, dwconv_w, dwconv_b, xconv);
-  k_xproj_dt<<<384, 256, 0, stream>>>(xconv, x_proj_w, dt_proj_w, dt_proj_b, dtp, Bp, Cp, u_t);
-  k_scan_part3<<<384, 256, 0, stream>>>(dtp, u_t, Bp, A_logs, hend, prodA);
-  k_scan_fix3<<<192, 256, 0, stream>>>(hend, prodA);
-  k_scan_y3<<<384, 256, 0, stream>>>(dtp, u_t, Bp, Cp, A_logs, Ds, prodA, ys_t);
-  k_combine_outproj<<<384, 256, 0, stream>>>(ys_t, z_t, out_norm_g, out_norm_b,
-                                             out_proj_w, x_cmaj, xv);
-  k_mlp<<<192, 256, 0, stream>>>(xv, ln2_g, ln2_b, fc1_w, fc1_b, fc2_w, fc2_b, (float*)d_out);
-}
+
+  hipError_t le = hipErrorUnknown;
+  int dev = 0;
+  if (hipGetDevice(&dev) == hipSuccess){
+    int numCU = 0, maxB = 0;
+    hipDeviceGetAttribute(&numCU, hipDeviceAttributeMultiprocessorCount, dev);
+    hipError_t oe = hipOccupancyMaxActiveBlocksPerMultiprocessor(&maxB, k_mega, 256, 0);
+    if (oe == hipSuccess && maxB > 0 && numCU > 0){
+      int grid = maxB * numCU; if (grid > 512) grid = 512;
+      if (grid >= 64){
+        void* args[] = { (void*)&Pm };
+        le = hipLaunchCooperativeKernel(k_mega, dim3(grid), dim3(256), args, 0u, stream);
+      }
+    }
+  }
+  if (le != hipSuccess){
+    k_p0 <<<96,   256, 0, stream>>>(Pm);
+    k_p1 <<<6*C3, 256, 0, stream>>>(Pm);
+    k_p2 <<<1536, 256, 0, stream>>>(Pm);
+    k_p3 <<<384,  256, 0, stream>>>(Pm);
+    k_p4 <<<6*CCH,256, 0, stream>>>(Pm);
+    k_p5 <<<576,  256, 0, stream>>>(Pm);
+    k_p6 <<<384,  256, 0, stream>>>(Pm);
+    k_p7 <<<384,  256, 0, stream>>>(Pm);
+    k_p8 <<<768,  256, 0, stream>>>(Pm);
+    k_p9 <<<384,  256, 0, stream>>>(Pm);
+    k_p10<<<384,  256, 0, stream>>>(Pm);
+    k_p11<<<192,  256, 0, stream>>>(Pm);
+    k_p12<<<384,  256, 0, stream>>>(Pm);
+    k_p13<<<384,  256, 0, stream>>>(Pm);
+    k_p14<<<192,  256, 0, stream>>>(Pm);
+  }
+}
```

After: 863.4 us. 173% more time.
